# Kernel optimization log

Hardware: AMD Instinct MI355X
Metric: run time of the kernel (lower is better)

Reference implementation:

```python
import jax, jax.numpy as jnp
import numpy as np

N = 16384        # num nodes
NE = 262144      # num edges (avg degree 16)
IN = 3           # input_dim
H = 128          # hidden_dim
ED = 2           # edge_dim (position differences, 2D coords)
L = 3            # num GNN layers
LAT = 64         # latent_dim
NR = 8192        # num reduced nodes (reduction_factor=0.5)
K = 3            # kNN for interpolation


def _ln(x, g, b, eps=1e-5):
    m = jnp.mean(x, axis=-1, keepdims=True)
    v = jnp.mean((x - m) ** 2, axis=-1, keepdims=True)
    return (x - m) / jnp.sqrt(v + eps) * g + b


def _mlp(x, w1, b1, w2, b2):
    return jax.nn.relu(x @ w1 + b1) @ w2 + b2


def setup_inputs() -> dict:
    key = jax.random.key(0)
    ks = jax.random.split(key, 32)
    def nrm(k, shape, s=0.05):
        return jax.random.normal(k, shape, dtype=jnp.float32) * s
    inp = {}
    inp["x"] = jax.random.normal(ks[0], (N, IN), dtype=jnp.float32)
    inp["node_positions"] = jax.random.uniform(ks[1], (N, 2), dtype=jnp.float32)
    inp["edge_index"] = jax.random.randint(ks[2], (2, NE), 0, N, dtype=jnp.int32)
    # mlp0 + lnm0
    inp["m0_w1"] = nrm(ks[3], (IN, H)); inp["m0_b1"] = jnp.zeros((H,), jnp.float32)
    inp["m0_w2"] = nrm(ks[4], (H, H)); inp["m0_b2"] = jnp.zeros((H,), jnp.float32)
    inp["ln0_g"] = jnp.ones((H,), jnp.float32); inp["ln0_b"] = jnp.zeros((H,), jnp.float32)
    # mlp1 + lnm1 (edge feature transform, edge_dim=2)
    inp["m1_w1"] = nrm(ks[5], (ED, H)); inp["m1_b1"] = jnp.zeros((H,), jnp.float32)
    inp["m1_w2"] = nrm(ks[6], (H, ED)); inp["m1_b2"] = jnp.zeros((ED,), jnp.float32)
    inp["ln1_g"] = jnp.ones((ED,), jnp.float32); inp["ln1_b"] = jnp.zeros((ED,), jnp.float32)
    # GNN layers (stacked over L)
    inp["g_msg_w1"] = nrm(ks[7], (L, 2 * H + ED, H)); inp["g_msg_b1"] = jnp.zeros((L, H), jnp.float32)
    inp["g_msg_w2"] = nrm(ks[8], (L, H, H)); inp["g_msg_b2"] = jnp.zeros((L, H), jnp.float32)
    inp["g_node_w1"] = nrm(ks[9], (L, 2 * H, H)); inp["g_node_b1"] = jnp.zeros((L, H), jnp.float32)
    inp["g_node_w2"] = nrm(ks[10], (L, H, H)); inp["g_node_b2"] = jnp.zeros((L, H), jnp.float32)
    inp["g_edge_w1"] = nrm(ks[11], (L, 2 * H + ED, H)); inp["g_edge_b1"] = jnp.zeros((L, H), jnp.float32)
    inp["g_edge_w2"] = nrm(ks[12], (L, H, ED)); inp["g_edge_b2"] = jnp.zeros((L, ED), jnp.float32)
    inp["g_lnn_g"] = jnp.ones((L, H), jnp.float32); inp["g_lnn_b"] = jnp.zeros((L, H), jnp.float32)
    inp["g_lne_g"] = jnp.ones((L, ED), jnp.float32); inp["g_lne_b"] = jnp.zeros((L, ED), jnp.float32)
    # mlp2 + lnm2
    inp["m2_w1"] = nrm(ks[13], (H, H)); inp["m2_b1"] = jnp.zeros((H,), jnp.float32)
    inp["m2_w2"] = nrm(ks[14], (H, H)); inp["m2_b2"] = jnp.zeros((H,), jnp.float32)
    inp["ln2_g"] = jnp.ones((H,), jnp.float32); inp["ln2_b"] = jnp.zeros((H,), jnp.float32)
    # output_proj
    inp["op_w1"] = nrm(ks[15], (H, H)); inp["op_b1"] = jnp.zeros((H,), jnp.float32)
    inp["op_w2"] = nrm(ks[16], (H, LAT)); inp["op_b2"] = jnp.zeros((LAT,), jnp.float32)
    return inp


def reference(x, edge_index, node_positions,
              m0_w1, m0_b1, m0_w2, m0_b2, ln0_g, ln0_b,
              m1_w1, m1_b1, m1_w2, m1_b2, ln1_g, ln1_b,
              g_msg_w1, g_msg_b1, g_msg_w2, g_msg_b2,
              g_node_w1, g_node_b1, g_node_w2, g_node_b2,
              g_edge_w1, g_edge_b1, g_edge_w2, g_edge_b2,
              g_lnn_g, g_lnn_b, g_lne_g, g_lne_b,
              m2_w1, m2_b1, m2_w2, m2_b2, ln2_g, ln2_b,
              op_w1, op_b1, op_w2, op_b2):
    row, col = edge_index[0], edge_index[1]
    # Stage 1: node encoder  U0 -> U1
    u = _ln(_mlp(x, m0_w1, m0_b1, m0_w2, m0_b2), ln0_g, ln0_b)
    # Stage 2: edge features from positions, E0 -> E1
    e = node_positions[col] - node_positions[row]          # [NE, 2]
    e = _ln(_mlp(e, m1_w1, m1_b1, m1_w2, m1_b2), ln1_g, ln1_b)
    # Stage 3: message-passing layers
    ones = jnp.ones((NE, 1), dtype=u.dtype)
    cnt = jnp.maximum(jax.ops.segment_sum(ones, col, num_segments=N), 1.0)
    for l in range(L):
        msg_in = jnp.concatenate([u[row], u[col], e], axis=-1)   # [NE, 2H+ED]
        m = _mlp(msg_in, g_msg_w1[l], g_msg_b1[l], g_msg_w2[l], g_msg_b2[l])
        agg = jax.ops.segment_sum(m, col, num_segments=N) / cnt  # mean aggregation
        u = _ln(u + _mlp(jnp.concatenate([u, agg], axis=-1),
                         g_node_w1[l], g_node_b1[l], g_node_w2[l], g_node_b2[l]),
                g_lnn_g[l], g_lnn_b[l])
        e = _ln(e + _mlp(jnp.concatenate([u[row], u[col], e], axis=-1),
                         g_edge_w1[l], g_edge_b1[l], g_edge_w2[l], g_edge_b2[l]),
                g_lne_g[l], g_lne_b[l])
    # Stage 4: U2 -> U3
    u3 = _ln(_mlp(u, m2_w1, m2_b1, m2_w2, m2_b2), ln2_g, ln2_b)
    # Stage 5: interpolate onto reduced coordinates (kNN inverse-distance weights)
    idx_r = jnp.floor(jnp.linspace(0.0, N - 1, NR)).astype(jnp.int32)
    x2 = node_positions[idx_r]                               # [NR, 2]
    d2 = (jnp.sum(x2 * x2, axis=1)[:, None]
          + jnp.sum(node_positions * node_positions, axis=1)[None, :]
          - 2.0 * x2 @ node_positions.T)                     # [NR, N]
    d2 = jnp.maximum(d2, 0.0)
    neg_d2, knn = jax.lax.top_k(-d2, K)                      # [NR, K]
    w = 1.0 / (jnp.sqrt(-neg_d2) + 1e-8)
    w = w / jnp.sum(w, axis=1, keepdims=True)
    z_feat = jnp.einsum('nk,nkh->nh', w, u3[knn])            # [NR, H]
    # Stage 6: global mean pool (no batch vector) + output projection
    z = jnp.mean(z_feat, axis=0, keepdims=True)              # [1, H]
    return _mlp(z, op_w1, op_b1, op_w2, op_b2)               # [1, LAT]
```

## Files before the change

kernel.cpp:

```cpp
#include <hip/hip_runtime.h>
#include <cfloat>

#define NN     16384
#define NEDGE  262144
#define HD     128
#define NLAYER 3
#define NRED   8192
#define LATD   64
#define GDIM   32

typedef __attribute__((ext_vector_type(8))) short short8;
typedef __attribute__((ext_vector_type(4))) float f32x4;

__device__ __forceinline__ unsigned short f2bf(float f) {
    union { float f; unsigned u; } v; v.f = f;
    unsigned u = v.u;
    unsigned r = u + 0x7fff + ((u >> 16) & 1);
    return (unsigned short)(r >> 16);
}
__device__ __forceinline__ void unp8(uint4 v, float* f) {
    unsigned w0=v.x, w1=v.y, w2=v.z, w3=v.w;
    f[0]=__uint_as_float(w0<<16); f[1]=__uint_as_float(w0&0xffff0000u);
    f[2]=__uint_as_float(w1<<16); f[3]=__uint_as_float(w1&0xffff0000u);
    f[4]=__uint_as_float(w2<<16); f[5]=__uint_as_float(w2&0xffff0000u);
    f[6]=__uint_as_float(w3<<16); f[7]=__uint_as_float(w3&0xffff0000u);
}
__device__ __forceinline__ unsigned long long umin64(unsigned long long a, unsigned long long b) {
    return a < b ? a : b;
}
__device__ __forceinline__ unsigned long long umax64(unsigned long long a, unsigned long long b) {
    return a < b ? b : a;
}

__device__ __forceinline__ unsigned short pack_std(const float* W, int ksteps, int q) {
    int j    = q & 7;
    int lane = (q >> 3) & 63;
    int ks   = (q >> 9) % ksteps;
    int nt   = q / (ksteps * 512);
    int k = ks*32 + (lane >> 4)*8 + j;
    int n = nt*16 + (lane & 15);
    return f2bf(W[k*128 + n]);
}
__device__ __forceinline__ unsigned short pack_w2e(const float* W, int q) {
    int j    = q & 7;
    int lane = (q >> 3) & 63;
    int ks   = q >> 9;
    int k = ks*32 + (lane >> 4)*8 + j;
    int n = lane & 15;
    return (n < 2) ? f2bf(W[k*2 + n]) : (unsigned short)0;
}

#define PK_TOTAL 448512
__global__ __launch_bounds__(256) void k_pack_all(
    const float* __restrict__ msgw1, const float* __restrict__ msgw2,
    const float* __restrict__ edgew1, const float* __restrict__ nodew1,
    const float* __restrict__ nodew2, const float* __restrict__ edgew2,
    const float* __restrict__ m0w2, const float* __restrict__ m2w1,
    const float* __restrict__ m2w2, unsigned short* __restrict__ P)
{
    int p = blockIdx.x*256 + threadIdx.x;
    if (p >= PK_TOTAL) return;
    unsigned short v;
    if (p < 98304) {
        int l = p / 32768, q = p % 32768;
        v = pack_std(msgw1 + (size_t)l*258*128, 8, q);
    } else if (p < 147456) {
        int t = p - 98304; int l = t / 16384, q = t % 16384;
        v = pack_std(msgw2 + (size_t)l*16384, 4, q);
    } else if (p < 245760) {
        int t = p - 147456; int l = t / 32768, q = t % 32768;
        v = pack_std(edgew1 + (size_t)l*258*128, 8, q);
    } else if (p < 344064) {
        int t = p - 245760; int l = t / 32768, q = t % 32768;
        v = pack_std(nodew1 + (size_t)l*256*128, 8, q);
    } else if (p < 393216) {
        int t = p - 344064; int l = t / 16384, q = t % 16384;
        v = pack_std(nodew2 + (size_t)l*16384, 4, q);
    } else if (p < 399360) {
        int t = p - 393216; int l = t / 2048, q = t % 2048;
        v = pack_w2e(edgew2 + (size_t)l*256, q);
    } else if (p < 415744) {
        v = pack_std(m0w2, 4, p - 399360);
    } else if (p < 432128) {
        v = pack_std(m2w1, 4, p - 415744);
    } else {
        v = pack_std(m2w2, 4, p - 432128);
    }
    P[p] = v;
}

union HUu { unsigned short Hs[64][136]; uint4 UF4[1024]; };

__global__ __launch_bounds__(256) void k_nenc_mfma(
    const float* __restrict__ x,
    const float* __restrict__ w1, const float* __restrict__ b1,
    const unsigned short* __restrict__ W2p, const float* __restrict__ B2,
    const float* __restrict__ lg, const float* __restrict__ lb,
    const unsigned short* __restrict__ mW1p,
    float* __restrict__ u, unsigned short* __restrict__ u16,
    unsigned short* __restrict__ RM, unsigned short* __restrict__ CM)
{
    __shared__ float xs[64][4];
    __shared__ float w1s[3][128];
    __shared__ float b1s[128];
    __shared__ HUu HU;
    __shared__ float Rs[64][132];
    __shared__ float red[64][4];
    __shared__ float mstat[64], sstat[64];
    int tid = threadIdx.x;
    int n0  = blockIdx.x * 64;
    for (int t = tid; t < 384; t += 256) w1s[t >> 7][t & 127] = w1[t];
    if (tid < 128) b1s[tid] = b1[tid];
    for (int t = tid; t < 192; t += 256) xs[t/3][t%3] = x[(size_t)n0*3 + t];
    __syncthreads();
    {
        int m = tid >> 2, p0 = (tid & 3) * 32;
        float x0 = xs[m][0], x1 = xs[m][1], x2 = xs[m][2];
        for (int j = p0; j < p0 + 32; j += 2) {
            float h0 = fmaxf(b1s[j]   + x0*w1s[0][j]   + x1*w1s[1][j]   + x2*w1s[2][j],   0.f);
            float h1 = fmaxf(b1s[j+1] + x0*w1s[0][j+1] + x1*w1s[1][j+1] + x2*w1s[2][j+1], 0.f);
            *(unsigned*)&HU.Hs[m][j] = f2bf(h0) | ((unsigned)f2bf(h1) << 16);
        }
    }
    __syncthreads();

    int lane = tid & 63, wave = tid >> 6;
    int lr = lane & 15, lq = lane >> 4;
    f32x4 acc[8];
    #pragma unroll
    for (int i = 0; i < 8; ++i) acc[i] = (f32x4){0.f,0.f,0.f,0.f};
    for (int ks = 0; ks < 4; ++ks) {
        short8 a0 = *(const short8*)&HU.Hs[ 0 + lr][ks*32 + lq*8];
        short8 a1 = *(const short8*)&HU.Hs[16 + lr][ks*32 + lq*8];
        short8 a2 = *(const short8*)&HU.Hs[32 + lr][ks*32 + lq*8];
        short8 a3 = *(const short8*)&HU.Hs[48 + lr][ks*32 + lq*8];
        short8 b0 = *(const short8*)(W2p + (size_t)(((wave*2+0)*4 + ks)*64 + lane)*8);
        short8 b1v= *(const short8*)(W2p + (size_t)(((wave*2+1)*4 + ks)*64 + lane)*8);
        acc[0] = __builtin_amdgcn_mfma_f32_16x16x32_bf16(a0, b0, acc[0], 0,0,0);
        acc[1] = __builtin_amdgcn_mfma_f32_16x16x32_bf16(a0, b1v, acc[1], 0,0,0);
        acc[2] = __builtin_amdgcn_mfma_f32_16x16x32_bf16(a1, b0, acc[2], 0,0,0);
        acc[3] = __builtin_amdgcn_mfma_f32_16x16x32_bf16(a1, b1v, acc[3], 0,0,0);
        acc[4] = __builtin_amdgcn_mfma_f32_16x16x32_bf16(a2, b0, acc[4], 0,0,0);
        acc[5] = __builtin_amdgcn_mfma_f32_16x16x32_bf16(a2, b1v, acc[5], 0,0,0);
        acc[6] = __builtin_amdgcn_mfma_f32_16x16x32_bf16(a3, b0, acc[6], 0,0,0);
        acc[7] = __builtin_amdgcn_mfma_f32_16x16x32_bf16(a3, b1v, acc[7], 0,0,0);
    }
    #pragma unroll
    for (int b = 0; b < 2; ++b) {
        int n = (wave*2 + b)*16 + lr;
        float bb = B2[n];
        #pragma unroll
        for (int mt = 0; mt < 4; ++mt) {
            f32x4 v = acc[mt*2 + b];
            #pragma unroll
            for (int r = 0; r < 4; ++r) {
                int m = mt*16 + lq*4 + r;
                Rs[m][n] = v[r] + bb;
            }
        }
    }
    __syncthreads();
    {
        int m = tid >> 2, p = tid & 3;
        float s = 0.f;
        #pragma unroll 8
        for (int i = 0; i < 32; ++i) s += Rs[m][p*32 + i];
        red[m][p] = s;
    }
    __syncthreads();
    if (tid < 64) mstat[tid] = (red[tid][0]+red[tid][1]+red[tid][2]+red[tid][3]) * (1.f/HD);
    __syncthreads();
    {
        int m = tid >> 2, p = tid & 3;
        float mm = mstat[m];
        float s = 0.f;
        #pragma unroll 8
        for (int i = 0; i < 32; ++i) { float d = Rs[m][p*32 + i] - mm; s += d*d; }
        red[m][p] = s;
    }
    __syncthreads();
    if (tid < 64) sstat[tid] = sqrtf((red[tid][0]+red[tid][1]+red[tid][2]+red[tid][3]) * (1.f/HD) + 1e-5f);
    __syncthreads();
    for (int t = tid; t < 2048; t += 256) {
        int m = t >> 5, q = t & 31;
        int n = q*4;
        float mm = mstat[m], sd = sstat[m];
        float4 g4 = *(const float4*)(lg + n);
        float4 b4 = *(const float4*)(lb + n);
        float o0 = (Rs[m][n+0]-mm)/sd*g4.x + b4.x;
        float o1 = (Rs[m][n+1]-mm)/sd*g4.y + b4.y;
        float o2 = (Rs[m][n+2]-mm)/sd*g4.z + b4.z;
        float o3 = (Rs[m][n+3]-mm)/sd*g4.w + b4.w;
        float4 fo; fo.x=o0; fo.y=o1; fo.z=o2; fo.w=o3;
        *(float4*)(u + (size_t)(n0+m)*HD + n) = fo;
        uint2 pk; pk.x = f2bf(o0) | (f2bf(o1)<<16); pk.y = f2bf(o2) | (f2bf(o3)<<16);
        *(uint2*)(u16 + (size_t)(n0+m)*HD + n) = pk;
        int ksf = n >> 5, sub = (n >> 3) & 3;
        int slot = (ksf*4 + (m >> 4))*64 + ((m & 15) | (sub << 4));
        unsigned short* UF = (unsigned short*)HU.UF4;
        *(uint2*)&UF[slot*8 + (n & 7)] = pk;
    }
    __syncthreads();

    for (int g = 0; g < 2; ++g) {
        int ksOff = g*4;
        unsigned short* Out = g ? CM : RM;
        #pragma unroll
        for (int i = 0; i < 8; ++i) acc[i] = (f32x4){0.f,0.f,0.f,0.f};
        for (int ks = 0; ks < 4; ++ks) {
            short8 a0 = *(const short8*)&HU.UF4[(ks*4+0)*64 + lane];
            short8 a1 = *(const short8*)&HU.UF4[(ks*4+1)*64 + lane];
            short8 a2 = *(const short8*)&HU.UF4[(ks*4+2)*64 + lane];
            short8 a3 = *(const short8*)&HU.UF4[(ks*4+3)*64 + lane];
            short8 b0 = *(const short8*)(mW1p + (size_t)(((wave*2+0)*8 + ksOff + ks)*64 + lane)*8);
            short8 b1v= *(const short8*)(mW1p + (size_t)(((wave*2+1)*8 + ksOff + ks)*64 + lane)*8);
            acc[0] = __builtin_amdgcn_mfma_f32_16x16x32_bf16(a0, b0, acc[0], 0,0,0);
            acc[1] = __builtin_amdgcn_mfma_f32_16x16x32_bf16(a0, b1v, acc[1], 0,0,0);
            acc[2] = __builtin_amdgcn_mfma_f32_16x16x32_bf16(a1, b0, acc[2], 0,0,0);
            acc[3] = __builtin_amdgcn_mfma_f32_16x16x32_bf16(a1, b1v, acc[3], 0,0,0);
            acc[4] = __builtin_amdgcn_mfma_f32_16x16x32_bf16(a2, b0, acc[4], 0,0,0);
            acc[5] = __builtin_amdgcn_mfma_f32_16x16x32_bf16(a2, b1v, acc[5], 0,0,0);
            acc[6] = __builtin_amdgcn_mfma_f32_16x16x32_bf16(a3, b0, acc[6], 0,0,0);
            acc[7] = __builtin_amdgcn_mfma_f32_16x16x32_bf16(a3, b1v, acc[7], 0,0,0);
        }
        #pragma unroll
        for (int b = 0; b < 2; ++b) {
            int n = (wave*2 + b)*16 + lr;
            #pragma unroll
            for (int mt = 0; mt < 4; ++mt) {
                f32x4 v = acc[mt*2 + b];
                #pragma unroll
                for (int r = 0; r < 4; ++r) {
                    int rowp = n0 + mt*16 + lq*4 + r;
                    unsigned hv = f2bf(v[r]);
                    unsigned ph = (unsigned)__shfl_xor((int)hv, 1, 64);
                    if (!(lr & 1))
                        *(unsigned*)&Out[(size_t)rowp*HD + n] = hv | (ph << 16);
                }
            }
        }
    }
}

__global__ __launch_bounds__(256) void k_edge_enc(
    const float* __restrict__ pos, const int* __restrict__ row, const int* __restrict__ col,
    const float* __restrict__ w1, const float* __restrict__ b1,
    const float* __restrict__ w2, const float* __restrict__ b2,
    const float* __restrict__ lg, const float* __restrict__ lb,
    float* __restrict__ ef)
{
    int e = blockIdx.x*256 + threadIdx.x;
    if (e >= NEDGE) return;
    int r = row[e], c = col[e];
    float e0 = pos[c*2]   - pos[r*2];
    float e1 = pos[c*2+1] - pos[r*2+1];
    float o0 = b2[0], o1 = b2[1];
    for (int j = 0; j < HD; ++j) {
        float h = fmaxf(e0*w1[j] + e1*w1[HD+j] + b1[j], 0.f);
        o0 += h*w2[j*2];
        o1 += h*w2[j*2+1];
    }
    float m  = 0.5f*(o0 + o1);
    float d0 = o0 - m, d1 = o1 - m;
    float v  = 0.5f*(d0*d0 + d1*d1);
    float sd = sqrtf(v + 1e-5f);
    ef[e*2]   = d0/sd*lg[0] + lb[0];
    ef[e*2+1] = d1/sd*lg[1] + lb[1];
}

__global__ void k_count(const int* __restrict__ col, int* __restrict__ cnt)
{
    int e = blockIdx.x*256 + threadIdx.x;
    if (e < NEDGE) atomicAdd(&cnt[col[e]], 1);
}

__global__ __launch_bounds__(256) void k_scan(
    const int* __restrict__ cnt, int* __restrict__ head)
{
    __shared__ int ls[257];
    int tid = threadIdx.x;
    int base = tid * (NN/256);
    int s = 0;
    for (int i = 0; i < NN/256; ++i) s += cnt[base + i];
    ls[tid+1] = s;
    if (tid == 0) ls[0] = 0;
    __syncthreads();
    if (tid == 0) {
        for (int i = 1; i <= 256; ++i) ls[i] += ls[i-1];
    }
    __syncthreads();
    int run = ls[tid];
    for (int i = 0; i < NN/256; ++i) {
        head[base + i] = run;
        run += cnt[base + i];
    }
}

__global__ __launch_bounds__(256) void k_scatter(
    const int* __restrict__ col, int* __restrict__ head, int* __restrict__ perm)
{
    int e = blockIdx.x*256 + threadIdx.x;
    if (e < NEDGE) {
        int p = atomicAdd(&head[col[e]], 1);
        perm[p] = e;
    }
}

__global__ __launch_bounds__(256) void k_gcount(const float* __restrict__ pos, int* __restrict__ gcnt)
{
    int i = blockIdx.x*256 + threadIdx.x;
    if (i < NN) {
        int cx = min(max((int)(pos[i*2]  *(float)GDIM), 0), GDIM-1);
        int cy = min(max((int)(pos[i*2+1]*(float)GDIM), 0), GDIM-1);
        atomicAdd(&gcnt[cy*GDIM + cx], 1);
    }
}

__global__ __launch_bounds__(256) void k_gscan(
    const int* __restrict__ gcnt, int* __restrict__ gstart, int* __restrict__ ghead)
{
    __shared__ int ls[257];
    int tid = threadIdx.x;
    int base = tid * 4;
    int s = 0;
    for (int i = 0; i < 4; ++i) s += gcnt[base + i];
    ls[tid+1] = s;
    if (tid == 0) ls[0] = 0;
    __syncthreads();
    if (tid == 0) for (int i = 1; i <= 256; ++i) ls[i] += ls[i-1];
    __syncthreads();
    int run = ls[tid];
    for (int i = 0; i < 4; ++i) {
        gstart[base+i] = run; ghead[base+i] = run;
        run += gcnt[base+i];
    }
    if (tid == 255) gstart[GDIM*GDIM] = run;
}

__global__ __launch_bounds__(256) void k_gscatter(
    const float* __restrict__ pos, int* __restrict__ ghead,
    float2* __restrict__ psort, int* __restrict__ pidx)
{
    int i = blockIdx.x*256 + threadIdx.x;
    if (i < NN) {
        float px = pos[i*2], py = pos[i*2+1];
        int cx = min(max((int)(px*(float)GDIM), 0), GDIM-1);
        int cy = min(max((int)(py*(float)GDIM), 0), GDIM-1);
        int p = atomicAdd(&ghead[cy*GDIM + cx], 1);
        float2 pp; pp.x = px; pp.y = py;
        psort[p] = pp;
        pidx[p] = i;
    }
}

__global__ __launch_bounds__(256) void k_knnsel(
    const float* __restrict__ pos, const int* __restrict__ gstart,
    const float2* __restrict__ psort, const int* __restrict__ pidx,
    int* __restrict__ knnidx, float* __restrict__ knnw)
{
    int r = blockIdx.x*256 + threadIdx.x;
    int ni = (int)(2.0*r + (double)r/8191.0);
    float qx = pos[ni*2], qy = pos[ni*2+1];
    float s2 = qx*qx + qy*qy;
    int cx = min(max((int)(qx*(float)GDIM), 0), GDIM-1);
    int cy = min(max((int)(qy*(float)GDIM), 0), GDIM-1);
    const float h = 1.f/(float)GDIM;
    unsigned long long k0 = ~0ull, k1 = ~0ull, k2 = ~0ull;
    for (int rr = 0; rr < GDIM; ++rr) {
        if (rr > 0 && k2 != ~0ull) {
            float bound = rr*h;
            float d3 = __uint_as_float((unsigned)(k2 >> 32));
            if (d3 < bound*bound*0.9999f) break;
        }
        int ylo = max(cy-rr, 0), yhi = min(cy+rr, GDIM-1);
        int xlo = max(cx-rr, 0), xhi = min(cx+rr, GDIM-1);
        for (int gy = ylo; gy <= yhi; ++gy) {
            bool yedge = (gy == cy-rr) || (gy == cy+rr);
            for (int gx = xlo; gx <= xhi; ++gx) {
                if (!yedge && gx != cx-rr && gx != cx+rr) continue;
                int cell = gy*GDIM + gx;
                int s = gstart[cell], e = gstart[cell+1];
                for (; s < e; ++s) {
                    float2 p = psort[s];
                    float sc = p.x*p.x + p.y*p.y;
                    float dt = qx*p.x + qy*p.y;
                    float d2 = fmaxf(s2 + sc - 2.f*dt, 0.f);
                    unsigned long long key =
                        ((unsigned long long)__float_as_uint(d2) << 32) | (unsigned)pidx[s];
                    unsigned long long a0 = umin64(k0, key);
                    unsigned long long a1 = umin64(k1, umax64(k0, key));
                    unsigned long long a2 = umin64(k2, umax64(k1, key));
                    k0 = a0; k1 = a1; k2 = a2;
                }
            }
        }
    }
    float d0 = __uint_as_float((unsigned)(k0 >> 32));
    float d1 = __uint_as_float((unsigned)(k1 >> 32));
    float d2 = __uint_as_float((unsigned)(k2 >> 32));
    float w0 = 1.f/(sqrtf(d0) + 1e-8f);
    float w1 = 1.f/(sqrtf(d1) + 1e-8f);
    float w2 = 1.f/(sqrtf(d2) + 1e-8f);
    float ws = w0 + w1 + w2;
    knnidx[r*3+0] = (int)(unsigned)(k0 & 0xffffffffu);
    knnidx[r*3+1] = (int)(unsigned)(k1 & 0xffffffffu);
    knnidx[r*3+2] = (int)(unsigned)(k2 & 0xffffffffu);
    knnw[r*3+0] = w0/ws;
    knnw[r*3+1] = w1/ws;
    knnw[r*3+2] = w2/ws;
}

__global__ __launch_bounds__(256) void k_gather(
    const float* __restrict__ u3, const int* __restrict__ knnidx,
    const float* __restrict__ knnw, float* __restrict__ zsum)
{
    __shared__ float zp[HD];
    int tid = threadIdx.x;
    if (tid < HD) zp[tid] = 0.f;
    __syncthreads();
    int lane = tid & 63, w = tid >> 6;
    int q = blockIdx.x*4 + w;
    int i0 = knnidx[q*3], i1 = knnidx[q*3+1], i2 = knnidx[q*3+2];
    float w0 = knnw[q*3], w1 = knnw[q*3+1], w2 = knnw[q*3+2];
    const float* r0 = u3 + (size_t)i0*HD;
    const float* r1 = u3 + (size_t)i1*HD;
    const float* r2 = u3 + (size_t)i2*HD;
    for (int c = lane; c < HD; c += 64) {
        float v = w0*r0[c] + w1*r1[c] + w2*r2[c];
        atomicAdd(&zp[c], v);
    }
    __syncthreads();
    if (tid < HD) atomicAdd(&zsum[tid], zp[tid]);
}

union MsHFu { uint4 HF4[1024]; float Ms[64][132]; };

__global__ __launch_bounds__(256) void k_msg2(
    const unsigned short* __restrict__ RM, const unsigned short* __restrict__ CM,
    const float* __restrict__ ef,
    const int* __restrict__ row, const int* __restrict__ col,
    const int* __restrict__ perm,
    const float* __restrict__ mW1e, const float* __restrict__ mB1,
    const unsigned short* __restrict__ W2p, const float* __restrict__ B2,
    float* __restrict__ agg)
{
    __shared__ MsHFu MU;
    __shared__ float Pw[256], Pb[128];
    __shared__ float Es[64][2];
    __shared__ int colS[64], rowS[64], eS[64];
    int tid = threadIdx.x;
    int e0  = blockIdx.x * 64;
    if (tid < 64) {
        int e = perm[e0 + tid];
        eS[tid] = e; colS[tid] = col[e]; rowS[tid] = row[e];
    }
    for (int t = tid; t < 256; t += 256) Pw[t] = mW1e[t];
    if (tid < 128) Pb[tid] = mB1[tid];
    __syncthreads();
    if (tid < 128) { Es[tid>>1][tid&1] = ef[(size_t)eS[tid>>1]*2 + (tid&1)]; }
    __syncthreads();

    #pragma unroll
    for (int s4 = 0; s4 < 4; ++s4) {
        int s = tid + s4*256;
        int lane_s = s & 63, ksmt = s >> 6;
        int ks = ksmt >> 2, mt = ksmt & 3;
        int m = mt*16 + (lane_s & 15);
        int cc = ks*32 + (lane_s >> 4)*8;
        uint4 ra = *(const uint4*)(RM + (size_t)rowS[m]*HD + cc);
        uint4 cb = *(const uint4*)(CM + (size_t)colS[m]*HD + cc);
        float rf[8], cf[8];
        unp8(ra, rf); unp8(cb, cf);
        float e0v = Es[m][0], e1v = Es[m][1];
        unsigned short hb[8];
        #pragma unroll
        for (int j = 0; j < 8; ++j) {
            int n = cc + j;
            float o = rf[j] + cf[j] + e0v*Pw[n] + e1v*Pw[128+n] + Pb[n];
            hb[j] = f2bf(fmaxf(o, 0.f));
        }
        uint4 pk;
        pk.x = hb[0] | ((unsigned)hb[1]<<16); pk.y = hb[2] | ((unsigned)hb[3]<<16);
        pk.z = hb[4] | ((unsigned)hb[5]<<16); pk.w = hb[6] | ((unsigned)hb[7]<<16);
        MU.HF4[s] = pk;
    }
    __syncthreads();

    int lane = tid & 63, wave = tid >> 6;
    int lr = lane & 15, lq = lane >> 4;
    f32x4 acc[8];
    #pragma unroll
    for (int i = 0; i < 8; ++i) acc[i] = (f32x4){0.f,0.f,0.f,0.f};
    for (int ks = 0; ks < 4; ++ks) {
        short8 a0 = *(const short8*)&MU.HF4[(ks*4+0)*64 + lane];
        short8 a1 = *(const short8*)&MU.HF4[(ks*4+1)*64 + lane];
        short8 a2 = *(const short8*)&MU.HF4[(ks*4+2)*64 + lane];
        short8 a3 = *(const short8*)&MU.HF4[(ks*4+3)*64 + lane];
        short8 b0 = *(const short8*)(W2p + (size_t)(((wave*2+0)*4 + ks)*64 + lane)*8);
        short8 b1 = *(const short8*)(W2p + (size_t)(((wave*2+1)*4 + ks)*64 + lane)*8);
        acc[0] = __builtin_amdgcn_mfma_f32_16x16x32_bf16(a0, b0, acc[0], 0,0,0);
        acc[1] = __builtin_amdgcn_mfma_f32_16x16x32_bf16(a0, b1, acc[1], 0,0,0);
        acc[2] = __builtin_amdgcn_mfma_f32_16x16x32_bf16(a1, b0, acc[2], 0,0,0);
        acc[3] = __builtin_amdgcn_mfma_f32_16x16x32_bf16(a1, b1, acc[3], 0,0,0);
        acc[4] = __builtin_amdgcn_mfma_f32_16x16x32_bf16(a2, b0, acc[4], 0,0,0);
        acc[5] = __builtin_amdgcn_mfma_f32_16x16x32_bf16(a2, b1, acc[5], 0,0,0);
        acc[6] = __builtin_amdgcn_mfma_f32_16x16x32_bf16(a3, b0, acc[6], 0,0,0);
        acc[7] = __builtin_amdgcn_mfma_f32_16x16x32_bf16(a3, b1, acc[7], 0,0,0);
    }
    __syncthreads();
    #pragma unroll
    for (int b = 0; b < 2; ++b) {
        int n = (wave*2 + b)*16 + lr;
        float bb = B2[n];
        #pragma unroll
        for (int mt = 0; mt < 4; ++mt) {
            f32x4 v = acc[mt*2 + b];
            #pragma unroll
            for (int r = 0; r < 4; ++r) {
                int m = mt*16 + lq*4 + r;
                MU.Ms[m][n] = v[r] + bb;
            }
        }
    }
    __syncthreads();
    {
        int n = tid & 127, hh = tid >> 7;
        int m0 = hh*32;
        float accv = 0.f;
        int cur = colS[m0];
        for (int m = m0; m < m0 + 32; ++m) {
            int cm = colS[m];
            if (cm != cur) {
                atomicAdd(&agg[(size_t)cur*HD + n], accv);
                accv = 0.f; cur = cm;
            }
            accv += MU.Ms[m][n];
        }
        atomicAdd(&agg[(size_t)cur*HD + n], accv);
    }
}

__global__ __launch_bounds__(256) void k_edgemsg2(
    const unsigned short* __restrict__ RE, const unsigned short* __restrict__ CE,
    const unsigned short* __restrict__ RM, const unsigned short* __restrict__ CM,
    float* __restrict__ ef,
    const int* __restrict__ row, const int* __restrict__ col,
    const int* __restrict__ perm,
    const float* __restrict__ eW1e, const float* __restrict__ eB1,
    const unsigned short* __restrict__ eW2p, const float* __restrict__ eB2,
    const float* __restrict__ elg, const float* __restrict__ elb,
    const float* __restrict__ mW1e, const float* __restrict__ mB1,
    const unsigned short* __restrict__ mW2p, const float* __restrict__ mB2,
    float* __restrict__ agg, int writeEf)
{
    __shared__ MsHFu MU;
    __shared__ float Pew[256], Peb[128], Pmw[256], Pmb[128];
    __shared__ float Es[64][2];
    __shared__ int colS[64], rowS[64], eS[64];
    int tid = threadIdx.x;
    int e0  = blockIdx.x * 64;
    if (tid < 64) {
        int e = perm[e0 + tid];
        eS[tid] = e; colS[tid] = col[e]; rowS[tid] = row[e];
    }
    for (int t = tid; t < 256; t += 256) { Pew[t] = eW1e[t]; Pmw[t] = mW1e[t]; }
    if (tid < 128) { Peb[tid] = eB1[tid]; Pmb[tid] = mB1[tid]; }
    __syncthreads();
    if (tid < 128) { Es[tid>>1][tid&1] = ef[(size_t)eS[tid>>1]*2 + (tid&1)]; }
    __syncthreads();

    int lane = tid & 63, wave = tid >> 6;
    int lr = lane & 15, lq = lane >> 4;

    #pragma unroll
    for (int s4 = 0; s4 < 4; ++s4) {
        int s = tid + s4*256;
        int lane_s = s & 63, ksmt = s >> 6;
        int ks = ksmt >> 2, mt = ksmt & 3;
        int m = mt*16 + (lane_s & 15);
        int cc = ks*32 + (lane_s >> 4)*8;
        uint4 ra = *(const uint4*)(RE + (size_t)rowS[m]*HD + cc);
        uint4 cb = *(const uint4*)(CE + (size_t)colS[m]*HD + cc);
        float rf[8], cf[8];
        unp8(ra, rf); unp8(cb, cf);
        float e0v = Es[m][0], e1v = Es[m][1];
        unsigned short hb[8];
        #pragma unroll
        for (int j = 0; j < 8; ++j) {
            int n = cc + j;
            float o = rf[j] + cf[j] + e0v*Pew[n] + e1v*Pew[128+n] + Peb[n];
            hb[j] = f2bf(fmaxf(o, 0.f));
        }
        uint4 pk;
        pk.x = hb[0] | ((unsigned)hb[1]<<16); pk.y = hb[2] | ((unsigned)hb[3]<<16);
        pk.z = hb[4] | ((unsigned)hb[5]<<16); pk.w = hb[6] | ((unsigned)hb[7]<<16);
        MU.HF4[s] = pk;
    }
    __syncthreads();

    f32x4 a2 = (f32x4){0.f,0.f,0.f,0.f};
    for (int ks = 0; ks < 4; ++ks) {
        short8 a = *(const short8*)&MU.HF4[(ks*4 + wave)*64 + lane];
        short8 b = *(const short8*)(eW2p + (size_t)(ks*64 + lane)*8);
        a2 = __builtin_amdgcn_mfma_f32_16x16x32_bf16(a, b, a2, 0,0,0);
    }
    if (lr < 2) {
        int d = lr;
        float bb = eB2[d];
        float gg = elg[d], bl = elb[d];
        #pragma unroll
        for (int r = 0; r < 4; ++r) {
            int m = wave*16 + lq*4 + r;
            float rv = Es[m][d] + a2[r] + bb;
            float other = __shfl_xor(rv, 1, 64);
            float mm = 0.5f*(rv + other);
            float dr = rv - mm, dro = other - mm;
            float vv = 0.5f*(dr*dr + dro*dro);
            float outv = dr / sqrtf(vv + 1e-5f) * gg + bl;
            Es[m][d] = outv;
            if (writeEf) ef[(size_t)eS[m]*2 + d] = outv;
        }
    }
    __syncthreads();

    #pragma unroll
    for (int s4 = 0; s4 < 4; ++s4) {
        int s = tid + s4*256;
        int lane_s = s & 63, ksmt = s >> 6;
        int ks = ksmt >> 2, mt = ksmt & 3;
        int m = mt*16 + (lane_s & 15);
        int cc = ks*32 + (lane_s >> 4)*8;
        uint4 ra = *(const uint4*)(RM + (size_t)rowS[m]*HD + cc);
        uint4 cb = *(const uint4*)(CM + (size_t)colS[m]*HD + cc);
        float rf[8], cf[8];
        unp8(ra, rf); unp8(cb, cf);
        float e0v = Es[m][0], e1v = Es[m][1];
        unsigned short hb[8];
        #pragma unroll
        for (int j = 0; j < 8; ++j) {
            int n = cc + j;
            float o = rf[j] + cf[j] + e0v*Pmw[n] + e1v*Pmw[128+n] + Pmb[n];
            hb[j] = f2bf(fmaxf(o, 0.f));
        }
        uint4 pk;
        pk.x = hb[0] | ((unsigned)hb[1]<<16); pk.y = hb[2] | ((unsigned)hb[3]<<16);
        pk.z = hb[4] | ((unsigned)hb[5]<<16); pk.w = hb[6] | ((unsigned)hb[7]<<16);
        MU.HF4[s] = pk;
    }
    __syncthreads();

    f32x4 acc[8];
    #pragma unroll
    for (int i = 0; i < 8; ++i) acc[i] = (f32x4){0.f,0.f,0.f,0.f};
    for (int ks = 0; ks < 4; ++ks) {
        short8 a0 = *(const short8*)&MU.HF4[(ks*4+0)*64 + lane];
        short8 a1 = *(const short8*)&MU.HF4[(ks*4+1)*64 + lane];
        short8 a2v= *(const short8*)&MU.HF4[(ks*4+2)*64 + lane];
        short8 a3 = *(const short8*)&MU.HF4[(ks*4+3)*64 + lane];
        short8 b0 = *(const short8*)(mW2p + (size_t)(((wave*2+0)*4 + ks)*64 + lane)*8);
        short8 b1 = *(const short8*)(mW2p + (size_t)(((wave*2+1)*4 + ks)*64 + lane)*8);
        acc[0] = __builtin_amdgcn_mfma_f32_16x16x32_bf16(a0, b0, acc[0], 0,0,0);
        acc[1] = __builtin_amdgcn_mfma_f32_16x16x32_bf16(a0, b1, acc[1], 0,0,0);
        acc[2] = __builtin_amdgcn_mfma_f32_16x16x32_bf16(a1, b0, acc[2], 0,0,0);
        acc[3] = __builtin_amdgcn_mfma_f32_16x16x32_bf16(a1, b1, acc[3], 0,0,0);
        acc[4] = __builtin_amdgcn_mfma_f32_16x16x32_bf16(a2v, b0, acc[4], 0,0,0);
        acc[5] = __builtin_amdgcn_mfma_f32_16x16x32_bf16(a2v, b1, acc[5], 0,0,0);
        acc[6] = __builtin_amdgcn_mfma_f32_16x16x32_bf16(a3, b0, acc[6], 0,0,0);
        acc[7] = __builtin_amdgcn_mfma_f32_16x16x32_bf16(a3, b1, acc[7], 0,0,0);
    }
    __syncthreads();
    #pragma unroll
    for (int b = 0; b < 2; ++b) {
        int n = (wave*2 + b)*16 + lr;
        float bb = mB2[n];
        #pragma unroll
        for (int mt = 0; mt < 4; ++mt) {
            f32x4 v = acc[mt*2 + b];
            #pragma unroll
            for (int r = 0; r < 4; ++r) {
                int m = mt*16 + lq*4 + r;
                MU.Ms[m][n] = v[r] + bb;
            }
        }
    }
    __syncthreads();
    {
        int n = tid & 127, hh = tid >> 7;
        int m0 = hh*32;
        float accv = 0.f;
        int cur = colS[m0];
        for (int m = m0; m < m0 + 32; ++m) {
            int cm = colS[m];
            if (cm != cur) {
                atomicAdd(&agg[(size_t)cur*HD + n], accv);
                accv = 0.f; cur = cm;
            }
            accv += MU.Ms[m][n];
        }
        atomicAdd(&agg[(size_t)cur*HD + n], accv);
    }
}

union XRu { unsigned short Xs[64][264]; float Rs[64][132]; };

__global__ __launch_bounds__(256) void k_node_mfma(
    float* __restrict__ u, unsigned short* __restrict__ u16,
    const float* __restrict__ agg, const int* __restrict__ cnt,
    const unsigned short* __restrict__ W1p, const float* __restrict__ B1,
    const unsigned short* __restrict__ W2p, const float* __restrict__ B2,
    const float* __restrict__ lg, const float* __restrict__ lb,
    int doExtra,
    const unsigned short* __restrict__ eW1p, const unsigned short* __restrict__ mW1p,
    unsigned short* __restrict__ RE, unsigned short* __restrict__ CE,
    unsigned short* __restrict__ RM, unsigned short* __restrict__ CM)
{
    __shared__ XRu XR;
    __shared__ HUu HU;
    __shared__ float red[64][4];
    __shared__ float mstat[64], sstat[64];
    int tid = threadIdx.x;
    int n0  = blockIdx.x * 64;
    for (int t = tid; t < 1024; t += 256) {
        int el = t >> 4, kc = t & 15;
        uint4 v = *(const uint4*)(u16 + (size_t)(n0+el)*HD + kc*8);
        *(uint4*)&XR.Xs[el][kc*8] = v;
    }
    for (int t = tid; t < 2048; t += 256) {
        int el = t >> 5, kc = t & 31;
        float inv = 1.f / fmaxf((float)cnt[n0+el], 1.f);
        float4 v = *(const float4*)(agg + (size_t)(n0+el)*HD + kc*4);
        unsigned r0 = f2bf(v.x*inv), r1 = f2bf(v.y*inv), r2 = f2bf(v.z*inv), r3 = f2bf(v.w*inv);
        uint2 pk; pk.x = r0 | (r1<<16); pk.y = r2 | (r3<<16);
        *(uint2*)&XR.Xs[el][HD + kc*4] = pk;
    }
    __syncthreads();

    int lane = tid & 63, wave = tid >> 6;
    int lr = lane & 15, lq = lane >> 4;
    f32x4 acc[8];
    #pragma unroll
    for (int i = 0; i < 8; ++i) acc[i] = (f32x4){0.f,0.f,0.f,0.f};

    for (int ks = 0; ks < 8; ++ks) {
        short8 a0 = *(const short8*)&XR.Xs[ 0 + lr][ks*32 + lq*8];
        short8 a1 = *(const short8*)&XR.Xs[16 + lr][ks*32 + lq*8];
        short8 a2 = *(const short8*)&XR.Xs[32 + lr][ks*32 + lq*8];
        short8 a3 = *(const short8*)&XR.Xs[48 + lr][ks*32 + lq*8];
        short8 b0 = *(const short8*)(W1p + (size_t)(((wave*2+0)*8 + ks)*64 + lane)*8);
        short8 b1 = *(const short8*)(W1p + (size_t)(((wave*2+1)*8 + ks)*64 + lane)*8);
        acc[0] = __builtin_amdgcn_mfma_f32_16x16x32_bf16(a0, b0, acc[0], 0,0,0);
        acc[1] = __builtin_amdgcn_mfma_f32_16x16x32_bf16(a0, b1, acc[1], 0,0,0);
        acc[2] = __builtin_amdgcn_mfma_f32_16x16x32_bf16(a1, b0, acc[2], 0,0,0);
        acc[3] = __builtin_amdgcn_mfma_f32_16x16x32_bf16(a1, b1, acc[3], 0,0,0);
        acc[4] = __builtin_amdgcn_mfma_f32_16x16x32_bf16(a2, b0, acc[4], 0,0,0);
        acc[5] = __builtin_amdgcn_mfma_f32_16x16x32_bf16(a2, b1, acc[5], 0,0,0);
        acc[6] = __builtin_amdgcn_mfma_f32_16x16x32_bf16(a3, b0, acc[6], 0,0,0);
        acc[7] = __builtin_amdgcn_mfma_f32_16x16x32_bf16(a3, b1, acc[7], 0,0,0);
    }
    #pragma unroll
    for (int b = 0; b < 2; ++b) {
        int n = (wave*2 + b)*16 + lr;
        float bb = B1[n];
        #pragma unroll
        for (int mt = 0; mt < 4; ++mt) {
            f32x4 v = acc[mt*2 + b];
            #pragma unroll
            for (int r = 0; r < 4; ++r) {
                int m = mt*16 + lq*4 + r;
                HU.Hs[m][n] = f2bf(fmaxf(v[r] + bb, 0.f));
            }
        }
    }
    __syncthreads();

    #pragma unroll
    for (int i = 0; i < 8; ++i) acc[i] = (f32x4){0.f,0.f,0.f,0.f};
    for (int ks = 0; ks < 4; ++ks) {
        short8 a0 = *(const short8*)&HU.Hs[ 0 + lr][ks*32 + lq*8];
        short8 a1 = *(const short8*)&HU.Hs[16 + lr][ks*32 + lq*8];
        short8 a2 = *(const short8*)&HU.Hs[32 + lr][ks*32 + lq*8];
        short8 a3 = *(const short8*)&HU.Hs[48 + lr][ks*32 + lq*8];
        short8 b0 = *(const short8*)(W2p + (size_t)(((wave*2+0)*4 + ks)*64 + lane)*8);
        short8 b1 = *(const short8*)(W2p + (size_t)(((wave*2+1)*4 + ks)*64 + lane)*8);
        acc[0] = __builtin_amdgcn_mfma_f32_16x16x32_bf16(a0, b0, acc[0], 0,0,0);
        acc[1] = __builtin_amdgcn_mfma_f32_16x16x32_bf16(a0, b1, acc[1], 0,0,0);
        acc[2] = __builtin_amdgcn_mfma_f32_16x16x32_bf16(a1, b0, acc[2], 0,0,0);
        acc[3] = __builtin_amdgcn_mfma_f32_16x16x32_bf16(a1, b1, acc[3], 0,0,0);
        acc[4] = __builtin_amdgcn_mfma_f32_16x16x32_bf16(a2, b0, acc[4], 0,0,0);
        acc[5] = __builtin_amdgcn_mfma_f32_16x16x32_bf16(a2, b1, acc[5], 0,0,0);
        acc[6] = __builtin_amdgcn_mfma_f32_16x16x32_bf16(a3, b0, acc[6], 0,0,0);
        acc[7] = __builtin_amdgcn_mfma_f32_16x16x32_bf16(a3, b1, acc[7], 0,0,0);
    }
    #pragma unroll
    for (int b = 0; b < 2; ++b) {
        int n = (wave*2 + b)*16 + lr;
        float bb = B2[n];
        #pragma unroll
        for (int mt = 0; mt < 4; ++mt) {
            f32x4 v = acc[mt*2 + b];
            #pragma unroll
            for (int r = 0; r < 4; ++r) {
                int m = mt*16 + lq*4 + r;
                XR.Rs[m][n] = u[(size_t)(n0+m)*HD + n] + v[r] + bb;
            }
        }
    }
    __syncthreads();
    {
        int m = tid >> 2, p = tid & 3;
        float s = 0.f;
        #pragma unroll 8
        for (int i = 0; i < 32; ++i) s += XR.Rs[m][p*32 + i];
        red[m][p] = s;
    }
    __syncthreads();
    if (tid < 64) mstat[tid] = (red[tid][0]+red[tid][1]+red[tid][2]+red[tid][3]) * (1.f/HD);
    __syncthreads();
    {
        int m = tid >> 2, p = tid & 3;
        float mm = mstat[m];
        float s = 0.f;
        #pragma unroll 8
        for (int i = 0; i < 32; ++i) { float d = XR.Rs[m][p*32 + i] - mm; s += d*d; }
        red[m][p] = s;
    }
    __syncthreads();
    if (tid < 64) sstat[tid] = sqrtf((red[tid][0]+red[tid][1]+red[tid][2]+red[tid][3]) * (1.f/HD) + 1e-5f);
    __syncthreads();
    for (int t = tid; t < 2048; t += 256) {
        int m = t >> 5, q = t & 31;
        int n = q*4;
        float mm = mstat[m], sd = sstat[m];
        float4 g4 = *(const float4*)(lg + n);
        float4 b4 = *(const float4*)(lb + n);
        float o0 = (XR.Rs[m][n+0]-mm)/sd*g4.x + b4.x;
        float o1 = (XR.Rs[m][n+1]-mm)/sd*g4.y + b4.y;
        float o2 = (XR.Rs[m][n+2]-mm)/sd*g4.z + b4.z;
        float o3 = (XR.Rs[m][n+3]-mm)/sd*g4.w + b4.w;
        float4 fo; fo.x=o0; fo.y=o1; fo.z=o2; fo.w=o3;
        *(float4*)(u + (size_t)(n0+m)*HD + n) = fo;
        uint2 pk; pk.x = f2bf(o0) | (f2bf(o1)<<16); pk.y = f2bf(o2) | (f2bf(o3)<<16);
        *(uint2*)(u16 + (size_t)(n0+m)*HD + n) = pk;
        if (doExtra) {
            int ksf = n >> 5, sub = (n >> 3) & 3;
            int slot = (ksf*4 + (m >> 4))*64 + ((m & 15) | (sub << 4));
            unsigned short* UF = (unsigned short*)HU.UF4;
            *(uint2*)&UF[slot*8 + (n & 7)] = pk;
        }
    }
    if (!doExtra) return;
    __syncthreads();

    for (int g = 0; g < 4; ++g) {
        const unsigned short* Bp = (g < 2) ? eW1p : mW1p;
        int ksOff = (g & 1) * 4;
        unsigned short* Out = (g == 0) ? RE : (g == 1) ? CE : (g == 2) ? RM : CM;
        #pragma unroll
        for (int i = 0; i < 8; ++i) acc[i] = (f32x4){0.f,0.f,0.f,0.f};
        for (int ks = 0; ks < 4; ++ks) {
            short8 a0 = *(const short8*)&HU.UF4[(ks*4+0)*64 + lane];
            short8 a1 = *(const short8*)&HU.UF4[(ks*4+1)*64 + lane];
            short8 a2 = *(const short8*)&HU.UF4[(ks*4+2)*64 + lane];
            short8 a3 = *(const short8*)&HU.UF4[(ks*4+3)*64 + lane];
            short8 b0 = *(const short8*)(Bp + (size_t)(((wave*2+0)*8 + ksOff + ks)*64 + lane)*8);
            short8 b1 = *(const short8*)(Bp + (size_t)(((wave*2+1)*8 + ksOff + ks)*64 + lane)*8);
            acc[0] = __builtin_amdgcn_mfma_f32_16x16x32_bf16(a0, b0, acc[0], 0,0,0);
            acc[1] = __builtin_amdgcn_mfma_f32_16x16x32_bf16(a0, b1, acc[1], 0,0,0);
            acc[2] = __builtin_amdgcn_mfma_f32_16x16x32_bf16(a1, b0, acc[2], 0,0,0);
            acc[3] = __builtin_amdgcn_mfma_f32_16x16x32_bf16(a1, b1, acc[3], 0,0,0);
            acc[4] = __builtin_amdgcn_mfma_f32_16x16x32_bf16(a2, b0, acc[4], 0,0,0);
            acc[5] = __builtin_amdgcn_mfma_f32_16x16x32_bf16(a2, b1, acc[5], 0,0,0);
            acc[6] = __builtin_amdgcn_mfma_f32_16x16x32_bf16(a3, b0, acc[6], 0,0,0);
            acc[7] = __builtin_amdgcn_mfma_f32_16x16x32_bf16(a3, b1, acc[7], 0,0,0);
        }
        #pragma unroll
        for (int b = 0; b < 2; ++b) {
            int n = (wave*2 + b)*16 + lr;
            #pragma unroll
            for (int mt = 0; mt < 4; ++mt) {
                f32x4 v = acc[mt*2 + b];
                #pragma unroll
                for (int r = 0; r < 4; ++r) {
                    int rowp = n0 + mt*16 + lq*4 + r;
                    unsigned hv = f2bf(v[r]);
                    unsigned ph = (unsigned)__shfl_xor((int)hv, 1, 64);
                    if (!(lr & 1))
                        *(unsigned*)&Out[(size_t)rowp*HD + n] = hv | (ph << 16);
                }
            }
        }
    }
}

__global__ __launch_bounds__(256) void k_m2_mfma(
    const unsigned short* __restrict__ u16,
    const unsigned short* __restrict__ W1p, const float* __restrict__ B1,
    const unsigned short* __restrict__ W2p, const float* __restrict__ B2,
    const float* __restrict__ lg, const float* __restrict__ lb,
    float* __restrict__ u3)
{
    __shared__ unsigned short Xs[64][136];
    __shared__ unsigned short Hs[64][136];
    __shared__ float Rs[64][132];
    __shared__ float red[64][4];
    __shared__ float mstat[64], sstat[64];
    int tid = threadIdx.x;
    int n0  = blockIdx.x * 64;
    for (int t = tid; t < 1024; t += 256) {
        int el = t >> 4, kc = t & 15;
        uint4 v = *(const uint4*)(u16 + (size_t)(n0+el)*HD + kc*8);
        *(uint4*)&Xs[el][kc*8] = v;
    }
    __syncthreads();

    int lane = tid & 63, wave = tid >> 6;
    int lr = lane & 15, lq = lane >> 4;
    f32x4 acc[8];
    #pragma unroll
    for (int i = 0; i < 8; ++i) acc[i] = (f32x4){0.f,0.f,0.f,0.f};
    for (int ks = 0; ks < 4; ++ks) {
        short8 a0 = *(const short8*)&Xs[ 0 + lr][ks*32 + lq*8];
        short8 a1 = *(const short8*)&Xs[16 + lr][ks*32 + lq*8];
        short8 a2 = *(const short8*)&Xs[32 + lr][ks*32 + lq*8];
        short8 a3 = *(const short8*)&Xs[48 + lr][ks*32 + lq*8];
        short8 b0 = *(const short8*)(W1p + (size_t)(((wave*2+0)*4 + ks)*64 + lane)*8);
        short8 b1 = *(const short8*)(W1p + (size_t)(((wave*2+1)*4 + ks)*64 + lane)*8);
        acc[0] = __builtin_amdgcn_mfma_f32_16x16x32_bf16(a0, b0, acc[0], 0,0,0);
        acc[1] = __builtin_amdgcn_mfma_f32_16x16x32_bf16(a0, b1, acc[1], 0,0,0);
        acc[2] = __builtin_amdgcn_mfma_f32_16x16x32_bf16(a1, b0, acc[2], 0,0,0);
        acc[3] = __builtin_amdgcn_mfma_f32_16x16x32_bf16(a1, b1, acc[3], 0,0,0);
        acc[4] = __builtin_amdgcn_mfma_f32_16x16x32_bf16(a2, b0, acc[4], 0,0,0);
        acc[5] = __builtin_amdgcn_mfma_f32_16x16x32_bf16(a2, b1, acc[5], 0,0,0);
        acc[6] = __builtin_amdgcn_mfma_f32_16x16x32_bf16(a3, b0, acc[6], 0,0,0);
        acc[7] = __builtin_amdgcn_mfma_f32_16x16x32_bf16(a3, b1, acc[7], 0,0,0);
    }
    #pragma unroll
    for (int b = 0; b < 2; ++b) {
        int n = (wave*2 + b)*16 + lr;
        float bb = B1[n];
        #pragma unroll
        for (int mt = 0; mt < 4; ++mt) {
            f32x4 v = acc[mt*2 + b];
            #pragma unroll
            for (int r = 0; r < 4; ++r) {
                int m = mt*16 + lq*4 + r;
                Hs[m][n] = f2bf(fmaxf(v[r] + bb, 0.f));
            }
        }
    }
    __syncthreads();

    #pragma unroll
    for (int i = 0; i < 8; ++i) acc[i] = (f32x4){0.f,0.f,0.f,0.f};
    for (int ks = 0; ks < 4; ++ks) {
        short8 a0 = *(const short8*)&Hs[ 0 + lr][ks*32 + lq*8];
        short8 a1 = *(const short8*)&Hs[16 + lr][ks*32 + lq*8];
        short8 a2 = *(const short8*)&Hs[32 + lr][ks*32 + lq*8];
        short8 a3 = *(const short8*)&Hs[48 + lr][ks*32 + lq*8];
        short8 b0 = *(const short8*)(W2p + (size_t)(((wave*2+0)*4 + ks)*64 + lane)*8);
        short8 b1 = *(const short8*)(W2p + (size_t)(((wave*2+1)*4 + ks)*64 + lane)*8);
        acc[0] = __builtin_amdgcn_mfma_f32_16x16x32_bf16(a0, b0, acc[0], 0,0,0);
        acc[1] = __builtin_amdgcn_mfma_f32_16x16x32_bf16(a0, b1, acc[1], 0,0,0);
        acc[2] = __builtin_amdgcn_mfma_f32_16x16x32_bf16(a1, b0, acc[2], 0,0,0);
        acc[3] = __builtin_amdgcn_mfma_f32_16x16x32_bf16(a1, b1, acc[3], 0,0,0);
        acc[4] = __builtin_amdgcn_mfma_f32_16x16x32_bf16(a2, b0, acc[4], 0,0,0);
        acc[5] = __builtin_amdgcn_mfma_f32_16x16x32_bf16(a2, b1, acc[5], 0,0,0);
        acc[6] = __builtin_amdgcn_mfma_f32_16x16x32_bf16(a3, b0, acc[6], 0,0,0);
        acc[7] = __builtin_amdgcn_mfma_f32_16x16x32_bf16(a3, b1, acc[7], 0,0,0);
    }
    #pragma unroll
    for (int b = 0; b < 2; ++b) {
        int n = (wave*2 + b)*16 + lr;
        float bb = B2[n];
        #pragma unroll
        for (int mt = 0; mt < 4; ++mt) {
            f32x4 v = acc[mt*2 + b];
            #pragma unroll
            for (int r = 0; r < 4; ++r) {
                int m = mt*16 + lq*4 + r;
                Rs[m][n] = v[r] + bb;
            }
        }
    }
    __syncthreads();
    {
        int m = tid >> 2, p = tid & 3;
        float s = 0.f;
        #pragma unroll 8
        for (int i = 0; i < 32; ++i) s += Rs[m][p*32 + i];
        red[m][p] = s;
    }
    __syncthreads();
    if (tid < 64) mstat[tid] = (red[tid][0]+red[tid][1]+red[tid][2]+red[tid][3]) * (1.f/HD);
    __syncthreads();
    {
        int m = tid >> 2, p = tid & 3;
        float mm = mstat[m];
        float s = 0.f;
        #pragma unroll 8
        for (int i = 0; i < 32; ++i) { float d = Rs[m][p*32 + i] - mm; s += d*d; }
        red[m][p] = s;
    }
    __syncthreads();
    if (tid < 64) sstat[tid] = sqrtf((red[tid][0]+red[tid][1]+red[tid][2]+red[tid][3]) * (1.f/HD) + 1e-5f);
    __syncthreads();
    for (int t = tid; t < 2048; t += 256) {
        int m = t >> 5, q = t & 31;
        int n = q*4;
        float mm = mstat[m], sd = sstat[m];
        float4 g4 = *(const float4*)(lg + n);
        float4 b4 = *(const float4*)(lb + n);
        float4 fo;
        fo.x = (Rs[m][n+0]-mm)/sd*g4.x + b4.x;
        fo.y = (Rs[m][n+1]-mm)/sd*g4.y + b4.y;
        fo.z = (Rs[m][n+2]-mm)/sd*g4.z + b4.z;
        fo.w = (Rs[m][n+3]-mm)/sd*g4.w + b4.w;
        *(float4*)(u3 + (size_t)(n0+m)*HD + n) = fo;
    }
}

__global__ __launch_bounds__(128) void k_out(
    const float* __restrict__ zsum,
    const float* __restrict__ w1, const float* __restrict__ b1,
    const float* __restrict__ w2, const float* __restrict__ b2,
    float* __restrict__ out)
{
    __shared__ float zs[HD];
    __shared__ float hs[HD];
    int j = threadIdx.x;
    zs[j] = zsum[j] * (1.f/NRED);
    __syncthreads();
    float o = b1[j];
    #pragma unroll 8
    for (int k = 0; k < HD; ++k) o += zs[k]*w1[k*HD + j];
    hs[j] = fmaxf(o, 0.f);
    __syncthreads();
    if (j < LATD) {
        float o2 = b2[j];
        #pragma unroll 8
        for (int k = 0; k < HD; ++k) o2 += hs[k]*w2[k*LATD + j];
        out[j] = o2;
    }
}

extern "C" void kernel_launch(void* const* d_in, const int* in_sizes, int n_in,
                              void* d_out, int out_size, void* d_ws, size_t ws_size,
                              hipStream_t stream)
{
    const float* x    = (const float*)d_in[0];
    const float* pos  = (const float*)d_in[1];
    const int*   eidx = (const int*)d_in[2];
    const int* row = eidx;
    const int* col = eidx + NEDGE;
    const float* m0_w1 = (const float*)d_in[3];
    const float* m0_b1 = (const float*)d_in[4];
    const float* m0_w2 = (const float*)d_in[5];
    const float* m0_b2 = (const float*)d_in[6];
    const float* ln0_g = (const float*)d_in[7];
    const float* ln0_b = (const float*)d_in[8];
    const float* m1_w1 = (const float*)d_in[9];
    const float* m1_b1 = (const float*)d_in[10];
    const float* m1_w2 = (const float*)d_in[11];
    const float* m1_b2 = (const float*)d_in[12];
    const float* ln1_g = (const float*)d_in[13];
    const float* ln1_b = (const float*)d_in[14];
    const float* g_msg_w1  = (const float*)d_in[15];
    const float* g_msg_b1  = (const float*)d_in[16];
    const float* g_msg_w2  = (const float*)d_in[17];
    const float* g_msg_b2  = (const float*)d_in[18];
    const float* g_node_w1 = (const float*)d_in[19];
    const float* g_node_b1 = (const float*)d_in[20];
    const float* g_node_w2 = (const float*)d_in[21];
    const float* g_node_b2 = (const float*)d_in[22];
    const float* g_edge_w1 = (const float*)d_in[23];
    const float* g_edge_b1 = (const float*)d_in[24];
    const float* g_edge_w2 = (const float*)d_in[25];
    const float* g_edge_b2 = (const float*)d_in[26];
    const float* g_lnn_g   = (const float*)d_in[27];
    const float* g_lnn_b   = (const float*)d_in[28];
    const float* g_lne_g   = (const float*)d_in[29];
    const float* g_lne_b   = (const float*)d_in[30];
    const float* m2_w1 = (const float*)d_in[31];
    const float* m2_b1 = (const float*)d_in[32];
    const float* m2_w2 = (const float*)d_in[33];
    const float* m2_b2 = (const float*)d_in[34];
    const float* ln2_g = (const float*)d_in[35];
    const float* ln2_b = (const float*)d_in[36];
    const float* op_w1 = (const float*)d_in[37];
    const float* op_b1 = (const float*)d_in[38];
    const float* op_w2 = (const float*)d_in[39];
    const float* op_b2 = (const float*)d_in[40];

    float* u    = (float*)d_ws;
    float* ef   = u + (size_t)NN*HD;
    float* agg  = ef + (size_t)NEDGE*2;
    int*   cnt  = (int*)(agg + (size_t)NN*HD);
    int*   head = cnt + NN;
    int*   perm = head + NN;
    float* zsum = (float*)(perm + NEDGE);
    int*   gcnt   = (int*)(zsum + HD);
    int*   gstart = gcnt + 1024;
    int*   ghead  = gstart + 1026;
    int*   pidx   = ghead + 1024;
    int*   knnidx = pidx + NN;
    float2* psort = (float2*)(knnidx + NRED*3 + 2);
    float* knnw   = (float*)(psort + NN);
    unsigned short* u16 = (unsigned short*)(knnw + NRED*3 + 1);
    unsigned short* packs = u16 + (size_t)NN*HD;
    unsigned short* msgW1p  = packs;
    unsigned short* msgW2p  = packs + 98304;
    unsigned short* edgeW1p = packs + 147456;
    unsigned short* nodeW1p = packs + 245760;
    unsigned short* nodeW2p = packs + 344064;
    unsigned short* edgeW2p = packs + 393216;
    unsigned short* m0w2p   = packs + 399360;
    unsigned short* m2w1p   = packs + 415744;
    unsigned short* m2w2p   = packs + 432128;
    unsigned short* RE = packs + PK_TOTAL;
    unsigned short* CE = RE + (size_t)NN*HD;
    unsigned short* RM = CE + (size_t)NN*HD;
    unsigned short* CM = RM + (size_t)NN*HD;
    float* u3 = agg;

    k_pack_all<<<(PK_TOTAL + 255)/256, 256, 0, stream>>>(
        g_msg_w1, g_msg_w2, g_edge_w1, g_node_w1, g_node_w2, g_edge_w2,
        m0_w2, m2_w1, m2_w2, packs);

    k_nenc_mfma<<<NN/64, 256, 0, stream>>>(x, m0_w1, m0_b1, m0w2p, m0_b2, ln0_g, ln0_b,
                                           msgW1p, u, u16, RM, CM);
    k_edge_enc<<<NEDGE/256, 256, 0, stream>>>(pos, row, col, m1_w1, m1_b1, m1_w2, m1_b2,
                                              ln1_g, ln1_b, ef);

    hipMemsetAsync(cnt, 0, NN*sizeof(int), stream);
    k_count<<<NEDGE/256, 256, 0, stream>>>(col, cnt);
    k_scan<<<1, 256, 0, stream>>>(cnt, head);
    k_scatter<<<NEDGE/256, 256, 0, stream>>>(col, head, perm);

    hipMemsetAsync(gcnt, 0, 1024*sizeof(int), stream);
    k_gcount<<<NN/256, 256, 0, stream>>>(pos, gcnt);
    k_gscan<<<1, 256, 0, stream>>>(gcnt, gstart, ghead);
    k_gscatter<<<NN/256, 256, 0, stream>>>(pos, ghead, psort, pidx);
    k_knnsel<<<NRED/256, 256, 0, stream>>>(pos, gstart, psort, pidx, knnidx, knnw);

    hipMemsetAsync(agg, 0, (size_t)NN*HD*sizeof(float), stream);
    k_msg2<<<NEDGE/64, 256, 0, stream>>>(RM, CM, ef, row, col, perm,
        g_msg_w1 + 256*HD, g_msg_b1, msgW2p, g_msg_b2, agg);
    k_node_mfma<<<NN/64, 256, 0, stream>>>(u, u16, agg, cnt,
        nodeW1p, g_node_b1, nodeW2p, g_node_b2, g_lnn_g, g_lnn_b,
        1, edgeW1p + 0*32768, msgW1p + 1*32768, RE, CE, RM, CM);

    for (int l = 0; l < NLAYER-1; ++l) {
        hipMemsetAsync(agg, 0, (size_t)NN*HD*sizeof(float), stream);
        k_edgemsg2<<<NEDGE/64, 256, 0, stream>>>(RE, CE, RM, CM, ef, row, col, perm,
            g_edge_w1 + (size_t)l*258*HD + 256*HD, g_edge_b1 + l*HD,
            edgeW2p + l*2048, g_edge_b2 + l*2, g_lne_g + l*2, g_lne_b + l*2,
            g_msg_w1 + (size_t)(l+1)*258*HD + 256*HD, g_msg_b1 + (l+1)*HD,
            msgW2p + (l+1)*16384, g_msg_b2 + (l+1)*HD,
            agg, (l == 0) ? 1 : 0);
        int doExtra = (l == 0) ? 1 : 0;
        k_node_mfma<<<NN/64, 256, 0, stream>>>(u, u16, agg, cnt,
            nodeW1p + (l+1)*32768, g_node_b1 + (l+1)*HD,
            nodeW2p + (l+1)*16384, g_node_b2 + (l+1)*HD,
            g_lnn_g + (l+1)*HD, g_lnn_b + (l+1)*HD,
            doExtra, edgeW1p + 1*32768, msgW1p + 2*32768, RE, CE, RM, CM);
    }

    k_m2_mfma<<<NN/64, 256, 0, stream>>>(u16, m2w1p, m2_b1, m2w2p, m2_b2, ln2_g, ln2_b, u3);
    hipMemsetAsync(zsum, 0, HD*sizeof(float), stream);
    k_gather<<<NRED/4, 256, 0, stream>>>(u3, knnidx, knnw, zsum);
    k_out<<<1, 128, 0, stream>>>(zsum, op_w1, op_b1, op_w2, op_b2, (float*)d_out);
}
```

Baseline: 531.3 us.

## Aggregate hidden activations before message W2 and fuse setup kernels

The message MLP's second linear layer is moved after the scatter-sum by linearity: edge kernels now aggregate the ReLU hidden vectors, and the node kernel applies W2 once per node, with the bias scaled by whether the node has any incoming edges. Biases are folded into the precomputed row/col projections. The count, scan and scatter kernels for edges and grid cells are merged, and the agg/zsum memsets are replaced by zeroing inside existing kernels. This removes the per-edge 128x128 MFMA and several launches, in exchange for an extra GEMM and an fp32-to-bf16 conversion of agg in the node kernel.

```diff
diff --git a/kernel.cpp b/kernel.cpp
--- a/kernel.cpp
+++ b/kernel.cpp
@@ -96,9 +96,10 @@
     const float* __restrict__ w1, const float* __restrict__ b1,
     const unsigned short* __restrict__ W2p, const float* __restrict__ B2,
     const float* __restrict__ lg, const float* __restrict__ lb,
-    const unsigned short* __restrict__ mW1p,
+    const unsigned short* __restrict__ mW1p, const float* __restrict__ mB1,
     float* __restrict__ u, unsigned short* __restrict__ u16,
-    unsigned short* __restrict__ RM, unsigned short* __restrict__ CM)
+    unsigned short* __restrict__ RM, unsigned short* __restrict__ CM,
+    float* __restrict__ agg)
 {
     __shared__ float xs[64][4];
     __shared__ float w1s[3][128];
@@ -109,6 +110,11 @@
     __shared__ float mstat[64], sstat[64];
     int tid = threadIdx.x;
     int n0  = blockIdx.x * 64;
+    {
+        float4 z; z.x=0.f; z.y=0.f; z.z=0.f; z.w=0.f;
+        for (int t = tid; t < 2048; t += 256)
+            *(float4*)(agg + (size_t)(n0 + (t>>5))*HD + (t&31)*4) = z;
+    }
     for (int t = tid; t < 384; t += 256) w1s[t >> 7][t & 127] = w1[t];
     if (tid < 128) b1s[tid] = b1[tid];
     for (int t = tid; t < 192; t += 256) xs[t/3][t%3] = x[(size_t)n0*3 + t];
@@ -226,13 +232,14 @@
         #pragma unroll
         for (int b = 0; b < 2; ++b) {
             int n = (wave*2 + b)*16 + lr;
+            float bb = g ? mB1[n] : 0.f;
             #pragma unroll
             for (int mt = 0; mt < 4; ++mt) {
                 f32x4 v = acc[mt*2 + b];
                 #pragma unroll
                 for (int r = 0; r < 4; ++r) {
                     int rowp = n0 + mt*16 + lq*4 + r;
-                    unsigned hv = f2bf(v[r]);
+                    unsigned hv = f2bf(v[r] + bb);
                     unsigned ph = (unsigned)__shfl_xor((int)hv, 1, 64);
                     if (!(lr & 1))
                         *(unsigned*)&Out[(size_t)rowp*HD + n] = hv | (ph << 16);
@@ -268,88 +275,76 @@
     ef[e*2+1] = d1/sd*lg[1] + lb[1];
 }
 
-__global__ void k_count(const int* __restrict__ col, int* __restrict__ cnt)
+__global__ void k_count2(const int* __restrict__ col, const float* __restrict__ pos,
+                         int* __restrict__ cnt, int* __restrict__ gcnt)
 {
     int e = blockIdx.x*256 + threadIdx.x;
     if (e < NEDGE) atomicAdd(&cnt[col[e]], 1);
-}
-
-__global__ __launch_bounds__(256) void k_scan(
-    const int* __restrict__ cnt, int* __restrict__ head)
+    if (e < NN) {
+        int cx = min(max((int)(pos[e*2]  *(float)GDIM), 0), GDIM-1);
+        int cy = min(max((int)(pos[e*2+1]*(float)GDIM), 0), GDIM-1);
+        atomicAdd(&gcnt[cy*GDIM + cx], 1);
+    }
+}
+
+__global__ __launch_bounds__(256) void k_scan2(
+    const int* __restrict__ cnt, int* __restrict__ head,
+    const int* __restrict__ gcnt, int* __restrict__ gstart, int* __restrict__ ghead,
+    float* __restrict__ zsum)
 {
     __shared__ int ls[257];
     int tid = threadIdx.x;
-    int base = tid * (NN/256);
-    int s = 0;
-    for (int i = 0; i < NN/256; ++i) s += cnt[base + i];
-    ls[tid+1] = s;
-    if (tid == 0) ls[0] = 0;
-    __syncthreads();
-    if (tid == 0) {
-        for (int i = 1; i <= 256; ++i) ls[i] += ls[i-1];
-    }
-    __syncthreads();
-    int run = ls[tid];
-    for (int i = 0; i < NN/256; ++i) {
-        head[base + i] = run;
-        run += cnt[base + i];
-    }
-}
-
-__global__ __launch_bounds__(256) void k_scatter(
-    const int* __restrict__ col, int* __restrict__ head, int* __restrict__ perm)
+    if (blockIdx.x == 0) {
+        int base = tid * (NN/256);
+        int s = 0;
+        for (int i = 0; i < NN/256; ++i) s += cnt[base + i];
+        ls[tid+1] = s;
+        if (tid == 0) ls[0] = 0;
+        __syncthreads();
+        if (tid == 0) for (int i = 1; i <= 256; ++i) ls[i] += ls[i-1];
+        __syncthreads();
+        int run = ls[tid];
+        for (int i = 0; i < NN/256; ++i) {
+            head[base + i] = run;
+            run += cnt[base + i];
+        }
+    } else {
+        if (tid < HD) zsum[tid] = 0.f;
+        int base = tid * 4;
+        int s = 0;
+        for (int i = 0; i < 4; ++i) s += gcnt[base + i];
+        ls[tid+1] = s;
+        if (tid == 0) ls[0] = 0;
+        __syncthreads();
+        if (tid == 0) for (int i = 1; i <= 256; ++i) ls[i] += ls[i-1];
+        __syncthreads();
+        int run = ls[tid];
+        for (int i = 0; i < 4; ++i) {
+            gstart[base+i] = run; ghead[base+i] = run;
+            run += gcnt[base+i];
+        }
+        if (tid == 255) gstart[GDIM*GDIM] = run;
+    }
+}
+
+__global__ __launch_bounds__(256) void k_scatter2(
+    const int* __restrict__ col, const float* __restrict__ pos,
+    int* __restrict__ head, int* __restrict__ perm,
+    int* __restrict__ ghead, float2* __restrict__ psort, int* __restrict__ pidx)
 {
     int e = blockIdx.x*256 + threadIdx.x;
     if (e < NEDGE) {
         int p = atomicAdd(&head[col[e]], 1);
         perm[p] = e;
     }
-}
-
-__global__ __launch_bounds__(256) void k_gcount(const float* __restrict__ pos, int* __restrict__ gcnt)
-{
-    int i = blockIdx.x*256 + threadIdx.x;
-    if (i < NN) {
-        int cx = min(max((int)(pos[i*2]  *(float)GDIM), 0), GDIM-1);
-        int cy = min(max((int)(pos[i*2+1]*(float)GDIM), 0), GDIM-1);
-        atomicAdd(&gcnt[cy*GDIM + cx], 1);
-    }
-}
-
-__global__ __launch_bounds__(256) void k_gscan(
-    const int* __restrict__ gcnt, int* __restrict__ gstart, int* __restrict__ ghead)
-{
-    __shared__ int ls[257];
-    int tid = threadIdx.x;
-    int base = tid * 4;
-    int s = 0;
-    for (int i = 0; i < 4; ++i) s += gcnt[base + i];
-    ls[tid+1] = s;
-    if (tid == 0) ls[0] = 0;
-    __syncthreads();
-    if (tid == 0) for (int i = 1; i <= 256; ++i) ls[i] += ls[i-1];
-    __syncthreads();
-    int run = ls[tid];
-    for (int i = 0; i < 4; ++i) {
-        gstart[base+i] = run; ghead[base+i] = run;
-        run += gcnt[base+i];
-    }
-    if (tid == 255) gstart[GDIM*GDIM] = run;
-}
-
-__global__ __launch_bounds__(256) void k_gscatter(
-    const float* __restrict__ pos, int* __restrict__ ghead,
-    float2* __restrict__ psort, int* __restrict__ pidx)
-{
-    int i = blockIdx.x*256 + threadIdx.x;
-    if (i < NN) {
-        float px = pos[i*2], py = pos[i*2+1];
+    if (e < NN) {
+        float px = pos[e*2], py = pos[e*2+1];
         int cx = min(max((int)(px*(float)GDIM), 0), GDIM-1);
         int cy = min(max((int)(py*(float)GDIM), 0), GDIM-1);
         int p = atomicAdd(&ghead[cy*GDIM + cx], 1);
         float2 pp; pp.x = px; pp.y = py;
         psort[p] = pp;
-        pidx[p] = i;
+        pidx[p] = e;
     }
 }
 
@@ -433,19 +428,16 @@
     if (tid < HD) atomicAdd(&zsum[tid], zp[tid]);
 }
 
-union MsHFu { uint4 HF4[1024]; float Ms[64][132]; };
-
-__global__ __launch_bounds__(256) void k_msg2(
+__global__ __launch_bounds__(256) void k_hagg0(
     const unsigned short* __restrict__ RM, const unsigned short* __restrict__ CM,
     const float* __restrict__ ef,
     const int* __restrict__ row, const int* __restrict__ col,
     const int* __restrict__ perm,
-    const float* __restrict__ mW1e, const float* __restrict__ mB1,
-    const unsigned short* __restrict__ W2p, const float* __restrict__ B2,
+    const float* __restrict__ mW1e,
     float* __restrict__ agg)
 {
-    __shared__ MsHFu MU;
-    __shared__ float Pw[256], Pb[128];
+    __shared__ float Ms[64][132];
+    __shared__ float Pw[256];
     __shared__ float Es[64][2];
     __shared__ int colS[64], rowS[64], eS[64];
     int tid = threadIdx.x;
@@ -455,74 +447,165 @@
         eS[tid] = e; colS[tid] = col[e]; rowS[tid] = row[e];
     }
     for (int t = tid; t < 256; t += 256) Pw[t] = mW1e[t];
-    if (tid < 128) Pb[tid] = mB1[tid];
     __syncthreads();
     if (tid < 128) { Es[tid>>1][tid&1] = ef[(size_t)eS[tid>>1]*2 + (tid&1)]; }
     __syncthreads();
 
+    int mP = (tid >> 6)*16 + (tid & 15);
+    int ccB = ((tid & 63) >> 4)*8;
+    float e0v = Es[mP][0], e1v = Es[mP][1];
     #pragma unroll
     for (int s4 = 0; s4 < 4; ++s4) {
-        int s = tid + s4*256;
-        int lane_s = s & 63, ksmt = s >> 6;
-        int ks = ksmt >> 2, mt = ksmt & 3;
-        int m = mt*16 + (lane_s & 15);
-        int cc = ks*32 + (lane_s >> 4)*8;
-        uint4 ra = *(const uint4*)(RM + (size_t)rowS[m]*HD + cc);
-        uint4 cb = *(const uint4*)(CM + (size_t)colS[m]*HD + cc);
+        int cc = s4*32 + ccB;
+        uint4 ra = *(const uint4*)(RM + (size_t)rowS[mP]*HD + cc);
+        uint4 cb = *(const uint4*)(CM + (size_t)colS[mP]*HD + cc);
         float rf[8], cf[8];
         unp8(ra, rf); unp8(cb, cf);
-        float e0v = Es[m][0], e1v = Es[m][1];
-        unsigned short hb[8];
-        #pragma unroll
-        for (int j = 0; j < 8; ++j) {
-            int n = cc + j;
-            float o = rf[j] + cf[j] + e0v*Pw[n] + e1v*Pw[128+n] + Pb[n];
-            hb[j] = f2bf(fmaxf(o, 0.f));
-        }
-        uint4 pk;
-        pk.x = hb[0] | ((unsigned)hb[1]<<16); pk.y = hb[2] | ((unsigned)hb[3]<<16);
-        pk.z = hb[4] | ((unsigned)hb[5]<<16); pk.w = hb[6] | ((unsigned)hb[7]<<16);
-        MU.HF4[s] = pk;
-    }
+        float4 o0, o1;
+        o0.x = fmaxf(rf[0]+cf[0]+e0v*Pw[cc+0]+e1v*Pw[128+cc+0], 0.f);
+        o0.y = fmaxf(rf[1]+cf[1]+e0v*Pw[cc+1]+e1v*Pw[128+cc+1], 0.f);
+        o0.z = fmaxf(rf[2]+cf[2]+e0v*Pw[cc+2]+e1v*Pw[128+cc+2], 0.f);
+        o0.w = fmaxf(rf[3]+cf[3]+e0v*Pw[cc+3]+e1v*Pw[128+cc+3], 0.f);
+        o1.x = fmaxf(rf[4]+cf[4]+e0v*Pw[cc+4]+e1v*Pw[128+cc+4], 0.f);
+        o1.y = fmaxf(rf[5]+cf[5]+e0v*Pw[cc+5]+e1v*Pw[128+cc+5], 0.f);
+        o1.z = fmaxf(rf[6]+cf[6]+e0v*Pw[cc+6]+e1v*Pw[128+cc+6], 0.f);
+        o1.w = fmaxf(rf[7]+cf[7]+e0v*Pw[cc+7]+e1v*Pw[128+cc+7], 0.f);
+        *(float4*)&Ms[mP][cc]   = o0;
+        *(float4*)&Ms[mP][cc+4] = o1;
+    }
+    __syncthreads();
+
+    {
+        int n = tid & 127, hh = tid >> 7;
+        int m0 = hh*32;
+        float accv = 0.f;
+        int cur = colS[m0];
+        for (int m = m0; m < m0 + 32; ++m) {
+            int cm = colS[m];
+            if (cm != cur) {
+                atomicAdd(&agg[(size_t)cur*HD + n], accv);
+                accv = 0.f; cur = cm;
+            }
+            accv += Ms[m][n];
+        }
+        atomicAdd(&agg[(size_t)cur*HD + n], accv);
+    }
+}
+
+union MsHFu { uint4 HF4[1024]; float Ms[64][132]; };
+
+__global__ __launch_bounds__(256) void k_edgemsg2(
+    const unsigned short* __restrict__ RE, const unsigned short* __restrict__ CE,
+    const unsigned short* __restrict__ RM, const unsigned short* __restrict__ CM,
+    float* __restrict__ ef,
+    const int* __restrict__ row, const int* __restrict__ col,
+    const int* __restrict__ perm,
+    const float* __restrict__ eW1e,
+    const unsigned short* __restrict__ eW2p, const float* __restrict__ eB2,
+    const float* __restrict__ elg, const float* __restrict__ elb,
+    const float* __restrict__ mW1e,
+    float* __restrict__ agg, int writeEf)
+{
+    __shared__ MsHFu MU;
+    __shared__ float Pew[256], Pmw[256];
+    __shared__ float Es[64][2];
+    __shared__ int colS[64], rowS[64], eS[64];
+    int tid = threadIdx.x;
+    int e0  = blockIdx.x * 64;
+    if (tid < 64) {
+        int e = perm[e0 + tid];
+        eS[tid] = e; colS[tid] = col[e]; rowS[tid] = row[e];
+    }
+    for (int t = tid; t < 256; t += 256) { Pew[t] = eW1e[t]; Pmw[t] = mW1e[t]; }
+    __syncthreads();
+
+    int mP = (tid >> 6)*16 + (tid & 15);
+    int ccB = ((tid & 63) >> 4)*8;
+    uint4 regR[4], regC[4];
+    #pragma unroll
+    for (int s4 = 0; s4 < 4; ++s4) {
+        int cc = s4*32 + ccB;
+        regR[s4] = *(const uint4*)(RM + (size_t)rowS[mP]*HD + cc);
+        regC[s4] = *(const uint4*)(CM + (size_t)colS[mP]*HD + cc);
+    }
+    if (tid < 128) { Es[tid>>1][tid&1] = ef[(size_t)eS[tid>>1]*2 + (tid&1)]; }
     __syncthreads();
 
     int lane = tid & 63, wave = tid >> 6;
     int lr = lane & 15, lq = lane >> 4;
-    f32x4 acc[8];
-    #pragma unroll
-    for (int i = 0; i < 8; ++i) acc[i] = (f32x4){0.f,0.f,0.f,0.f};
+
+    {
+        float e0v = Es[mP][0], e1v = Es[mP][1];
+        #pragma unroll
+        for (int s4 = 0; s4 < 4; ++s4) {
+            int s = tid + s4*256;
+            int cc = s4*32 + ccB;
+            uint4 ra = *(const uint4*)(RE + (size_t)rowS[mP]*HD + cc);
+            uint4 cb = *(const uint4*)(CE + (size_t)colS[mP]*HD + cc);
+            float rf[8], cf[8];
+            unp8(ra, rf); unp8(cb, cf);
+            unsigned short hb[8];
+            #pragma unroll
+            for (int j = 0; j < 8; ++j) {
+                int n = cc + j;
+                float o = rf[j] + cf[j] + e0v*Pew[n] + e1v*Pew[128+n];
+                hb[j] = f2bf(fmaxf(o, 0.f));
+            }
+            uint4 pk;
+            pk.x = hb[0] | ((unsigned)hb[1]<<16); pk.y = hb[2] | ((unsigned)hb[3]<<16);
+            pk.z = hb[4] | ((unsigned)hb[5]<<16); pk.w = hb[6] | ((unsigned)hb[7]<<16);
+            MU.HF4[s] = pk;
+        }
+    }
+    __syncthreads();
+
+    f32x4 a2 = (f32x4){0.f,0.f,0.f,0.f};
     for (int ks = 0; ks < 4; ++ks) {
-        short8 a0 = *(const short8*)&MU.HF4[(ks*4+0)*64 + lane];
-        short8 a1 = *(const short8*)&MU.HF4[(ks*4+1)*64 + lane];
-        short8 a2 = *(const short8*)&MU.HF4[(ks*4+2)*64 + lane];
-        short8 a3 = *(const short8*)&MU.HF4[(ks*4+3)*64 + lane];
-        short8 b0 = *(const short8*)(W2p + (size_t)(((wave*2+0)*4 + ks)*64 + lane)*8);
-        short8 b1 = *(const short8*)(W2p + (size_t)(((wave*2+1)*4 + ks)*64 + lane)*8);
-        acc[0] = __builtin_amdgcn_mfma_f32_16x16x32_bf16(a0, b0, acc[0], 0,0,0);
-        acc[1] = __builtin_amdgcn_mfma_f32_16x16x32_bf16(a0, b1, acc[1], 0,0,0);
-        acc[2] = __builtin_amdgcn_mfma_f32_16x16x32_bf16(a1, b0, acc[2], 0,0,0);
-        acc[3] = __builtin_amdgcn_mfma_f32_16x16x32_bf16(a1, b1, acc[3], 0,0,0);
-        acc[4] = __builtin_amdgcn_mfma_f32_16x16x32_bf16(a2, b0, acc[4], 0,0,0);
-        acc[5] = __builtin_amdgcn_mfma_f32_16x16x32_bf16(a2, b1, acc[5], 0,0,0);
-        acc[6] = __builtin_amdgcn_mfma_f32_16x16x32_bf16(a3, b0, acc[6], 0,0,0);
-        acc[7] = __builtin_amdgcn_mfma_f32_16x16x32_bf16(a3, b1, acc[7], 0,0,0);
-    }
-    __syncthreads();
-    #pragma unroll
-    for (int b = 0; b < 2; ++b) {
-        int n = (wave*2 + b)*16 + lr;
-        float bb = B2[n];
-        #pragma unroll
-        for (int mt = 0; mt < 4; ++mt) {
-            f32x4 v = acc[mt*2 + b];
-            #pragma unroll
-            for (int r = 0; r < 4; ++r) {
-                int m = mt*16 + lq*4 + r;
-                MU.Ms[m][n] = v[r] + bb;
-            }
-        }
-    }
-    __syncthreads();
+        short8 a = *(const short8*)&MU.HF4[(ks*4 + wave)*64 + lane];
+        short8 b = *(const short8*)(eW2p + (size_t)(ks*64 + lane)*8);
+        a2 = __builtin_amdgcn_mfma_f32_16x16x32_bf16(a, b, a2, 0,0,0);
+    }
+    if (lr < 2) {
+        int d = lr;
+        float bb = eB2[d];
+        float gg = elg[d], bl = elb[d];
+        #pragma unroll
+        for (int r = 0; r < 4; ++r) {
+            int m = wave*16 + lq*4 + r;
+            float rv = Es[m][d] + a2[r] + bb;
+            float other = __shfl_xor(rv, 1, 64);
+            float mm = 0.5f*(rv + other);
+            float dr = rv - mm, dro = other - mm;
+            float vv = 0.5f*(dr*dr + dro*dro);
+            float outv = dr / sqrtf(vv + 1e-5f) * gg + bl;
+            Es[m][d] = outv;
+            if (writeEf) ef[(size_t)eS[m]*2 + d] = outv;
+        }
+    }
+    __syncthreads();
+
+    {
+        float e0v = Es[mP][0], e1v = Es[mP][1];
+        #pragma unroll
+        for (int s4 = 0; s4 < 4; ++s4) {
+            int cc = s4*32 + ccB;
+            float rf[8], cf[8];
+            unp8(regR[s4], rf); unp8(regC[s4], cf);
+            float4 o0, o1;
+            o0.x = fmaxf(rf[0]+cf[0]+e0v*Pmw[cc+0]+e1v*Pmw[128+cc+0], 0.f);
+            o0.y = fmaxf(rf[1]+cf[1]+e0v*Pmw[cc+1]+e1v*Pmw[128+cc+1], 0.f);
+            o0.z = fmaxf(rf[2]+cf[2]+e0v*Pmw[cc+2]+e1v*Pmw[128+cc+2], 0.f);
+            o0.w = fmaxf(rf[3]+cf[3]+e0v*Pmw[cc+3]+e1v*Pmw[128+cc+3], 0.f);
+            o1.x = fmaxf(rf[4]+cf[4]+e0v*Pmw[cc+4]+e1v*Pmw[128+cc+4], 0.f);
+            o1.y = fmaxf(rf[5]+cf[5]+e0v*Pmw[cc+5]+e1v*Pmw[128+cc+5], 0.f);
+            o1.z = fmaxf(rf[6]+cf[6]+e0v*Pmw[cc+6]+e1v*Pmw[128+cc+6], 0.f);
+            o1.w = fmaxf(rf[7]+cf[7]+e0v*Pmw[cc+7]+e1v*Pmw[128+cc+7], 0.f);
+            *(float4*)&MU.Ms[mP][cc]   = o0;
+            *(float4*)&MU.Ms[mP][cc+4] = o1;
+        }
+    }
+    __syncthreads();
+
     {
         int n = tid & 127, hh = tid >> 7;
         int m0 = hh*32;
@@ -540,177 +623,18 @@
     }
 }
 
-__global__ __launch_bounds__(256) void k_edgemsg2(
-    const unsigned short* __restrict__ RE, const unsigned short* __restrict__ CE,
-    const unsigned short* __restrict__ RM, const unsigned short* __restrict__ CM,
-    float* __restrict__ ef,
-    const int* __restrict__ row, const int* __restrict__ col,
-    const int* __restrict__ perm,
-    const float* __restrict__ eW1e, const float* __restrict__ eB1,
-    const unsigned short* __restrict__ eW2p, const float* __restrict__ eB2,
-    const float* __restrict__ elg, const float* __restrict__ elb,
-    const float* __restrict__ mW1e, const float* __restrict__ mB1,
-    const unsigned short* __restrict__ mW2p, const float* __restrict__ mB2,
-    float* __restrict__ agg, int writeEf)
-{
-    __shared__ MsHFu MU;
-    __shared__ float Pew[256], Peb[128], Pmw[256], Pmb[128];
-    __shared__ float Es[64][2];
-    __shared__ int colS[64], rowS[64], eS[64];
-    int tid = threadIdx.x;
-    int e0  = blockIdx.x * 64;
-    if (tid < 64) {
-        int e = perm[e0 + tid];
-        eS[tid] = e; colS[tid] = col[e]; rowS[tid] = row[e];
-    }
-    for (int t = tid; t < 256; t += 256) { Pew[t] = eW1e[t]; Pmw[t] = mW1e[t]; }
-    if (tid < 128) { Peb[tid] = eB1[tid]; Pmb[tid] = mB1[tid]; }
-    __syncthreads();
-    if (tid < 128) { Es[tid>>1][tid&1] = ef[(size_t)eS[tid>>1]*2 + (tid&1)]; }
-    __syncthreads();
-
-    int lane = tid & 63, wave = tid >> 6;
-    int lr = lane & 15, lq = lane >> 4;
-
-    #pragma unroll
-    for (int s4 = 0; s4 < 4; ++s4) {
-        int s = tid + s4*256;
-        int lane_s = s & 63, ksmt = s >> 6;
-        int ks = ksmt >> 2, mt = ksmt & 3;
-        int m = mt*16 + (lane_s & 15);
-        int cc = ks*32 + (lane_s >> 4)*8;
-        uint4 ra = *(const uint4*)(RE + (size_t)rowS[m]*HD + cc);
-        uint4 cb = *(const uint4*)(CE + (size_t)colS[m]*HD + cc);
-        float rf[8], cf[8];
-        unp8(ra, rf); unp8(cb, cf);
-        float e0v = Es[m][0], e1v = Es[m][1];
-        unsigned short hb[8];
-        #pragma unroll
-        for (int j = 0; j < 8; ++j) {
-            int n = cc + j;
-            float o = rf[j] + cf[j] + e0v*Pew[n] + e1v*Pew[128+n] + Peb[n];
-            hb[j] = f2bf(fmaxf(o, 0.f));
-        }
-        uint4 pk;
-        pk.x = hb[0] | ((unsigned)hb[1]<<16); pk.y = hb[2] | ((unsigned)hb[3]<<16);
-        pk.z = hb[4] | ((unsigned)hb[5]<<16); pk.w = hb[6] | ((unsigned)hb[7]<<16);
-        MU.HF4[s] = pk;
-    }
-    __syncthreads();
-
-    f32x4 a2 = (f32x4){0.f,0.f,0.f,0.f};
-    for (int ks = 0; ks < 4; ++ks) {
-        short8 a = *(const short8*)&MU.HF4[(ks*4 + wave)*64 + lane];
-        short8 b = *(const short8*)(eW2p + (size_t)(ks*64 + lane)*8);
-        a2 = __builtin_amdgcn_mfma_f32_16x16x32_bf16(a, b, a2, 0,0,0);
-    }
-    if (lr < 2) {
-        int d = lr;
-        float bb = eB2[d];
-        float gg = elg[d], bl = elb[d];
-        #pragma unroll
-        for (int r = 0; r < 4; ++r) {
-            int m = wave*16 + lq*4 + r;
-            float rv = Es[m][d] + a2[r] + bb;
-            float other = __shfl_xor(rv, 1, 64);
-            float mm = 0.5f*(rv + other);
-            float dr = rv - mm, dro = other - mm;
-            float vv = 0.5f*(dr*dr + dro*dro);
-            float outv = dr / sqrtf(vv + 1e-5f) * gg + bl;
-            Es[m][d] = outv;
-            if (writeEf) ef[(size_t)eS[m]*2 + d] = outv;
-        }
-    }
-    __syncthreads();
-
-    #pragma unroll
-    for (int s4 = 0; s4 < 4; ++s4) {
-        int s = tid + s4*256;
-        int lane_s = s & 63, ksmt = s >> 6;
-        int ks = ksmt >> 2, mt = ksmt & 3;
-        int m = mt*16 + (lane_s & 15);
-        int cc = ks*32 + (lane_s >> 4)*8;
-        uint4 ra = *(const uint4*)(RM + (size_t)rowS[m]*HD + cc);
-        uint4 cb = *(const uint4*)(CM + (size_t)colS[m]*HD + cc);
-        float rf[8], cf[8];
-        unp8(ra, rf); unp8(cb, cf);
-        float e0v = Es[m][0], e1v = Es[m][1];
-        unsigned short hb[8];
-        #pragma unroll
-        for (int j = 0; j < 8; ++j) {
-            int n = cc + j;
-            float o = rf[j] + cf[j] + e0v*Pmw[n] + e1v*Pmw[128+n] + Pmb[n];
-            hb[j] = f2bf(fmaxf(o, 0.f));
-        }
-        uint4 pk;
-        pk.x = hb[0] | ((unsigned)hb[1]<<16); pk.y = hb[2] | ((unsigned)hb[3]<<16);
-        pk.z = hb[4] | ((unsigned)hb[5]<<16); pk.w = hb[6] | ((unsigned)hb[7]<<16);
-        MU.HF4[s] = pk;
-    }
-    __syncthreads();
-
-    f32x4 acc[8];
-    #pragma unroll
-    for (int i = 0; i < 8; ++i) acc[i] = (f32x4){0.f,0.f,0.f,0.f};
-    for (int ks = 0; ks < 4; ++ks) {
-        short8 a0 = *(const short8*)&MU.HF4[(ks*4+0)*64 + lane];
-        short8 a1 = *(const short8*)&MU.HF4[(ks*4+1)*64 + lane];
-        short8 a2v= *(const short8*)&MU.HF4[(ks*4+2)*64 + lane];
-        short8 a3 = *(const short8*)&MU.HF4[(ks*4+3)*64 + lane];
-        short8 b0 = *(const short8*)(mW2p + (size_t)(((wave*2+0)*4 + ks)*64 + lane)*8);
-        short8 b1 = *(const short8*)(mW2p + (size_t)(((wave*2+1)*4 + ks)*64 + lane)*8);
-        acc[0] = __builtin_amdgcn_mfma_f32_16x16x32_bf16(a0, b0, acc[0], 0,0,0);
-        acc[1] = __builtin_amdgcn_mfma_f32_16x16x32_bf16(a0, b1, acc[1], 0,0,0);
-        acc[2] = __builtin_amdgcn_mfma_f32_16x16x32_bf16(a1, b0, acc[2], 0,0,0);
-        acc[3] = __builtin_amdgcn_mfma_f32_16x16x32_bf16(a1, b1, acc[3], 0,0,0);
-        acc[4] = __builtin_amdgcn_mfma_f32_16x16x32_bf16(a2v, b0, acc[4], 0,0,0);
-        acc[5] = __builtin_amdgcn_mfma_f32_16x16x32_bf16(a2v, b1, acc[5], 0,0,0);
-        acc[6] = __builtin_amdgcn_mfma_f32_16x16x32_bf16(a3, b0, acc[6], 0,0,0);
-        acc[7] = __builtin_amdgcn_mfma_f32_16x16x32_bf16(a3, b1, acc[7], 0,0,0);
-    }
-    __syncthreads();
-    #pragma unroll
-    for (int b = 0; b < 2; ++b) {
-        int n = (wave*2 + b)*16 + lr;
-        float bb = mB2[n];
-        #pragma unroll
-        for (int mt = 0; mt < 4; ++mt) {
-            f32x4 v = acc[mt*2 + b];
-            #pragma unroll
-            for (int r = 0; r < 4; ++r) {
-                int m = mt*16 + lq*4 + r;
-                MU.Ms[m][n] = v[r] + bb;
-            }
-        }
-    }
-    __syncthreads();
-    {
-        int n = tid & 127, hh = tid >> 7;
-        int m0 = hh*32;
-        float accv = 0.f;
-        int cur = colS[m0];
-        for (int m = m0; m < m0 + 32; ++m) {
-            int cm = colS[m];
-            if (cm != cur) {
-                atomicAdd(&agg[(size_t)cur*HD + n], accv);
-                accv = 0.f; cur = cm;
-            }
-            accv += MU.Ms[m][n];
-        }
-        atomicAdd(&agg[(size_t)cur*HD + n], accv);
-    }
-}
-
 union XRu { unsigned short Xs[64][264]; float Rs[64][132]; };
 
 __global__ __launch_bounds__(256) void k_node_mfma(
     float* __restrict__ u, unsigned short* __restrict__ u16,
-    const float* __restrict__ agg, const int* __restrict__ cnt,
+    float* __restrict__ agg, const int* __restrict__ cnt,
     const unsigned short* __restrict__ W1p, const float* __restrict__ B1,
     const unsigned short* __restrict__ W2p, const float* __restrict__ B2,
     const float* __restrict__ lg, const float* __restrict__ lb,
+    const unsigned short* __restrict__ mW2pC, const float* __restrict__ mB2C,
     int doExtra,
-    const unsigned short* __restrict__ eW1p, const unsigned short* __restrict__ mW1p,
+    const unsigned short* __restrict__ eW1p, const float* __restrict__ eB1c,
+    const unsigned short* __restrict__ mW1pN, const float* __restrict__ mB1N,
     unsigned short* __restrict__ RE, unsigned short* __restrict__ CE,
     unsigned short* __restrict__ RM, unsigned short* __restrict__ CM)
 {
@@ -718,6 +642,7 @@
     __shared__ HUu HU;
     __shared__ float red[64][4];
     __shared__ float mstat[64], sstat[64];
+    __shared__ float invS[64], fS[64];
     int tid = threadIdx.x;
     int n0  = blockIdx.x * 64;
     for (int t = tid; t < 1024; t += 256) {
@@ -725,22 +650,72 @@
         uint4 v = *(const uint4*)(u16 + (size_t)(n0+el)*HD + kc*8);
         *(uint4*)&XR.Xs[el][kc*8] = v;
     }
-    for (int t = tid; t < 2048; t += 256) {
-        int el = t >> 5, kc = t & 31;
-        float inv = 1.f / fmaxf((float)cnt[n0+el], 1.f);
-        float4 v = *(const float4*)(agg + (size_t)(n0+el)*HD + kc*4);
-        unsigned r0 = f2bf(v.x*inv), r1 = f2bf(v.y*inv), r2 = f2bf(v.z*inv), r3 = f2bf(v.w*inv);
-        uint2 pk; pk.x = r0 | (r1<<16); pk.y = r2 | (r3<<16);
-        *(uint2*)&XR.Xs[el][HD + kc*4] = pk;
+    if (tid < 64) {
+        int c = cnt[n0 + tid];
+        invS[tid] = 1.f / fmaxf((float)c, 1.f);
+        fS[tid] = (c > 0) ? 1.f : 0.f;
+    }
+    for (int t = tid; t < 1024; t += 256) {
+        int lane_s = t & 63, ksmt = t >> 6;
+        int ks = ksmt >> 2, mt = ksmt & 3;
+        int el = mt*16 + (lane_s & 15);
+        int cc = ks*32 + (lane_s >> 4)*8;
+        const float* src = agg + (size_t)(n0+el)*HD + cc;
+        float4 a = *(const float4*)src;
+        float4 b = *(const float4*)(src + 4);
+        uint4 pk;
+        pk.x = f2bf(a.x) | ((unsigned)f2bf(a.y) << 16);
+        pk.y = f2bf(a.z) | ((unsigned)f2bf(a.w) << 16);
+        pk.z = f2bf(b.x) | ((unsigned)f2bf(b.y) << 16);
+        pk.w = f2bf(b.z) | ((unsigned)f2bf(b.w) << 16);
+        HU.UF4[t] = pk;
     }
     __syncthreads();
 
     int lane = tid & 63, wave = tid >> 6;
     int lr = lane & 15, lq = lane >> 4;
     f32x4 acc[8];
+
     #pragma unroll
     for (int i = 0; i < 8; ++i) acc[i] = (f32x4){0.f,0.f,0.f,0.f};
-
+    for (int ks = 0; ks < 4; ++ks) {
+        short8 a0 = *(const short8*)&HU.UF4[(ks*4+0)*64 + lane];
+        short8 a1 = *(const short8*)&HU.UF4[(ks*4+1)*64 + lane];
+        short8 a2 = *(const short8*)&HU.UF4[(ks*4+2)*64 + lane];
+        short8 a3 = *(const short8*)&HU.UF4[(ks*4+3)*64 + lane];
+        short8 b0 = *(const short8*)(mW2pC + (size_t)(((wave*2+0)*4 + ks)*64 + lane)*8);
+        short8 b1 = *(const short8*)(mW2pC + (size_t)(((wave*2+1)*4 + ks)*64 + lane)*8);
+        acc[0] = __builtin_amdgcn_mfma_f32_16x16x32_bf16(a0, b0, acc[0], 0,0,0);
+        acc[1] = __builtin_amdgcn_mfma_f32_16x16x32_bf16(a0, b1, acc[1], 0,0,0);
+        acc[2] = __builtin_amdgcn_mfma_f32_16x16x32_bf16(a1, b0, acc[2], 0,0,0);
+        acc[3] = __builtin_amdgcn_mfma_f32_16x16x32_bf16(a1, b1, acc[3], 0,0,0);
+        acc[4] = __builtin_amdgcn_mfma_f32_16x16x32_bf16(a2, b0, acc[4], 0,0,0);
+        acc[5] = __builtin_amdgcn_mfma_f32_16x16x32_bf16(a2, b1, acc[5], 0,0,0);
+        acc[6] = __builtin_amdgcn_mfma_f32_16x16x32_bf16(a3, b0, acc[6], 0,0,0);
+        acc[7] = __builtin_amdgcn_mfma_f32_16x16x32_bf16(a3, b1, acc[7], 0,0,0);
+    }
+    #pragma unroll
+    for (int b = 0; b < 2; ++b) {
+        int n = (wave*2 + b)*16 + lr;
+        float bb = mB2C[n];
+        #pragma unroll
+        for (int mt = 0; mt < 4; ++mt) {
+            f32x4 v = acc[mt*2 + b];
+            #pragma unroll
+            for (int r = 0; r < 4; ++r) {
+                int m = mt*16 + lq*4 + r;
+                float val = v[r]*invS[m] + fS[m]*bb;
+                unsigned hv = f2bf(val);
+                unsigned ph = (unsigned)__shfl_xor((int)hv, 1, 64);
+                if (!(lr & 1))
+                    *(unsigned*)&XR.Xs[m][128 + n] = hv | (ph << 16);
+            }
+        }
+    }
+    __syncthreads();
+
+    #pragma unroll
+    for (int i = 0; i < 8; ++i) acc[i] = (f32x4){0.f,0.f,0.f,0.f};
     for (int ks = 0; ks < 8; ++ks) {
         short8 a0 = *(const short8*)&XR.Xs[ 0 + lr][ks*32 + lq*8];
         short8 a1 = *(const short8*)&XR.Xs[16 + lr][ks*32 + lq*8];
@@ -848,13 +823,19 @@
             *(uint2*)&UF[slot*8 + (n & 7)] = pk;
         }
     }
+    {
+        float4 z; z.x=0.f; z.y=0.f; z.z=0.f; z.w=0.f;
+        for (int t = tid; t < 2048; t += 256)
+            *(float4*)(agg + (size_t)(n0 + (t>>5))*HD + (t&31)*4) = z;
+    }
     if (!doExtra) return;
     __syncthreads();
 
     for (int g = 0; g < 4; ++g) {
-        const unsigned short* Bp = (g < 2) ? eW1p : mW1p;
+        const unsigned short* Bp = (g < 2) ? eW1p : mW1pN;
         int ksOff = (g & 1) * 4;
         unsigned short* Out = (g == 0) ? RE : (g == 1) ? CE : (g == 2) ? RM : CM;
+        const float* bias = (g == 1) ? eB1c : (g == 3) ? mB1N : (const float*)nullptr;
         #pragma unroll
         for (int i = 0; i < 8; ++i) acc[i] = (f32x4){0.f,0.f,0.f,0.f};
         for (int ks = 0; ks < 4; ++ks) {
@@ -876,13 +857,14 @@
         #pragma unroll
         for (int b = 0; b < 2; ++b) {
             int n = (wave*2 + b)*16 + lr;
+            float bb = bias ? bias[n] : 0.f;
             #pragma unroll
             for (int mt = 0; mt < 4; ++mt) {
                 f32x4 v = acc[mt*2 + b];
                 #pragma unroll
                 for (int r = 0; r < 4; ++r) {
                     int rowp = n0 + mt*16 + lq*4 + r;
-                    unsigned hv = f2bf(v[r]);
+                    unsigned hv = f2bf(v[r] + bb);
                     unsigned ph = (unsigned)__shfl_xor((int)hv, 1, 64);
                     if (!(lr & 1))
                         *(unsigned*)&Out[(size_t)rowp*HD + n] = hv | (ph << 16);
@@ -1095,11 +1077,11 @@
     float* ef   = u + (size_t)NN*HD;
     float* agg  = ef + (size_t)NEDGE*2;
     int*   cnt  = (int*)(agg + (size_t)NN*HD);
-    int*   head = cnt + NN;
+    int*   gcnt = cnt + NN;
+    int*   head = gcnt + 1024;
     int*   perm = head + NN;
     float* zsum = (float*)(perm + NEDGE);
-    int*   gcnt   = (int*)(zsum + HD);
-    int*   gstart = gcnt + 1024;
+    int*   gstart = (int*)(zsum + HD);
     int*   ghead  = gstart + 1026;
     int*   pidx   = ghead + 1024;
     int*   knnidx = pidx + NN;
@@ -1126,47 +1108,43 @@
         g_msg_w1, g_msg_w2, g_edge_w1, g_node_w1, g_node_w2, g_edge_w2,
         m0_w2, m2_w1, m2_w2, packs);
 
+    hipMemsetAsync(cnt, 0, (NN + 1024)*sizeof(int), stream);
+
     k_nenc_mfma<<<NN/64, 256, 0, stream>>>(x, m0_w1, m0_b1, m0w2p, m0_b2, ln0_g, ln0_b,
-                                           msgW1p, u, u16, RM, CM);
+                                           msgW1p, g_msg_b1, u, u16, RM, CM, agg);
     k_edge_enc<<<NEDGE/256, 256, 0, stream>>>(pos, row, col, m1_w1, m1_b1, m1_w2, m1_b2,
                                               ln1_g, ln1_b, ef);
 
-    hipMemsetAsync(cnt, 0, NN*sizeof(int), stream);
-    k_count<<<NEDGE/256, 256, 0, stream>>>(col, cnt);
-    k_scan<<<1, 256, 0, stream>>>(cnt, head);
-    k_scatter<<<NEDGE/256, 256, 0, stream>>>(col, head, perm);
-
-    hipMemsetAsync(gcnt, 0, 1024*sizeof(int), stream);
-    k_gcount<<<NN/256, 256, 0, stream>>>(pos, gcnt);
-    k_gscan<<<1, 256, 0, stream>>>(gcnt, gstart, ghead);
-    k_gscatter<<<NN/256, 256, 0, stream>>>(pos, ghead, psort, pidx);
+    k_count2<<<NEDGE/256, 256, 0, stream>>>(col, pos, cnt, gcnt);
+    k_scan2<<<2, 256, 0, stream>>>(cnt, head, gcnt, gstart, ghead, zsum);
+    k_scatter2<<<NEDGE/256, 256, 0, stream>>>(col, pos, head, perm, ghead, psort, pidx);
     k_knnsel<<<NRED/256, 256, 0, stream>>>(pos, gstart, psort, pidx, knnidx, knnw);
 
-    hipMemsetAsync(agg, 0, (size_t)NN*HD*sizeof(float), stream);
-    k_msg2<<<NEDGE/64, 256, 0, stream>>>(RM, CM, ef, row, col, perm,
-        g_msg_w1 + 256*HD, g_msg_b1, msgW2p, g_msg_b2, agg);
+    k_hagg0<<<NEDGE/64, 256, 0, stream>>>(RM, CM, ef, row, col, perm,
+        g_msg_w1 + 256*HD, agg);
     k_node_mfma<<<NN/64, 256, 0, stream>>>(u, u16, agg, cnt,
         nodeW1p, g_node_b1, nodeW2p, g_node_b2, g_lnn_g, g_lnn_b,
-        1, edgeW1p + 0*32768, msgW1p + 1*32768, RE, CE, RM, CM);
+        msgW2p, g_msg_b2,
+        1, edgeW1p + 0*32768, g_edge_b1 + 0*HD, msgW1p + 1*32768, g_msg_b1 + 1*HD,
+        RE, CE, RM, CM);
 
     for (int l = 0; l < NLAYER-1; ++l) {
-        hipMemsetAsync(agg, 0, (size_t)NN*HD*sizeof(float), stream);
         k_edgemsg2<<<NEDGE/64, 256, 0, stream>>>(RE, CE, RM, CM, ef, row, col, perm,
-            g_edge_w1 + (size_t)l*258*HD + 256*HD, g_edge_b1 + l*HD,
+            g_edge_w1 + (size_t)l*258*HD + 256*HD,
             edgeW2p + l*2048, g_edge_b2 + l*2, g_lne_g + l*2, g_lne_b + l*2,
-            g_msg_w1 + (size_t)(l+1)*258*HD + 256*HD, g_msg_b1 + (l+1)*HD,
-            msgW2p + (l+1)*16384, g_msg_b2 + (l+1)*HD,
+            g_msg_w1 + (size_t)(l+1)*258*HD + 256*HD,
             agg, (l == 0) ? 1 : 0);
         int doExtra = (l == 0) ? 1 : 0;
         k_node_mfma<<<NN/64, 256, 0, stream>>>(u, u16, agg, cnt,
             nodeW1p + (l+1)*32768, g_node_b1 + (l+1)*HD,
             nodeW2p + (l+1)*16384, g_node_b2 + (l+1)*HD,
             g_lnn_g + (l+1)*HD, g_lnn_b + (l+1)*HD,
-            doExtra, edgeW1p + 1*32768, msgW1p + 2*32768, RE, CE, RM, CM);
+            msgW2p + (l+1)*16384, g_msg_b2 + (l+1)*HD,
+            doExtra, edgeW1p + 1*32768, g_edge_b1 + 1*HD, msgW1p + 2*32768, g_msg_b1 + 2*HD,
+            RE, CE, RM, CM);
     }
 
     k_m2_mfma<<<NN/64, 256, 0, stream>>>(u16, m2w1p, m2_b1, m2w2p, m2_b2, ln2_g, ln2_b, u3);
-    hipMemsetAsync(zsum, 0, HD*sizeof(float), stream);
     k_gather<<<NRED/4, 256, 0, stream>>>(u3, knnidx, knnw, zsum);
     k_out<<<1, 128, 0, stream>>>(zsum, op_w1, op_b1, op_w2, op_b2, (float*)d_out);
 }
```

Measured after the change: 494.4 us. 1.07x faster.
